# Kernel tuning notes

Hardware: AMD Instinct MI355X
Metric: run time of the kernel (lower is better)

The kernel has to match this reference:

```python
import jax, jax.numpy as jnp
import numpy as np

B, N, NID, V, GH, PHI, RHO = 8, 256, 64, 128, 128, 256, 128
BN = B * N
EPS = 1e-5


def _layernorm(x, g, b):
    m = jnp.mean(x, axis=-1, keepdims=True)
    v = jnp.var(x, axis=-1, keepdims=True)
    return (x - m) * jax.lax.rsqrt(v + EPS) * g + b


def _edges(A):
    # dense adjacency -> flat batched edge list, exactly as mask.nonzero() ordering
    bidx = jnp.arange(B)[:, None, None]
    ii = jnp.arange(N)[None, :, None]
    jj = jnp.arange(N)[None, None, :]
    src = jnp.broadcast_to(bidx * N + ii, (B, N, N)).reshape(-1)  # edge_index[0] = b*N+i
    tgt = jnp.broadcast_to(bidx * N + jj, (B, N, N)).reshape(-1)  # edge_index[1] = b*N+j
    w = A.reshape(-1)
    valid = w != 0
    rel = (w > 0).astype(jnp.int32)
    return src, tgt, w, valid, rel


def _rgcn(H, src, tgt, valid, rel, Wrel, Wroot, bias):
    # torch_geometric RGCNConv: mean aggregation per relation at target + root + bias
    x_src = H[src]  # (E, d) gather
    out = H @ Wroot + bias
    for r in range(2):
        m = (valid & (rel == r)).astype(H.dtype)  # (E,)
        s = jax.ops.segment_sum(x_src * m[:, None], tgt, num_segments=BN)
        c = jax.ops.segment_sum(m, tgt, num_segments=BN)
        out = out + (s / jnp.maximum(c, 1.0)[:, None]) @ Wrel[r]
    return out


def setup_inputs() -> dict:
    key = jax.random.key(0)
    ks = jax.random.split(key, 24)
    p = lambda k, shape: jax.random.normal(k, shape, dtype=jnp.float32) * 0.02
    z = lambda *shape: jnp.zeros(shape, jnp.float32)
    return {
        "A": jax.random.normal(ks[0], (B, N, N), dtype=jnp.float32),
        "X": jax.random.normal(ks[1], (B, N, NID), dtype=jnp.float32),
        "home_mask": (jax.random.uniform(ks[2], (B, N)) > 0.5).astype(jnp.float32),
        "emb1_w": p(ks[3], (NID, V)), "emb1_b": z(V),
        "emb2_w": p(ks[4], (V, V)), "emb2_b": z(V),
        "rgcn_w_0": p(ks[5], (2, V, GH)), "rgcn_root_0": p(ks[6], (V, GH)), "rgcn_bias_0": z(GH),
        "lina_w_0": p(ks[7], (GH, GH)), "lina_b_0": z(GH),
        "linb_w_0": p(ks[8], (GH, GH)), "linb_b_0": z(GH),
        "rgcn_w_1": p(ks[9], (2, GH, GH)), "rgcn_root_1": p(ks[10], (GH, GH)), "rgcn_bias_1": z(GH),
        "lina_w_1": p(ks[11], (GH, GH)), "lina_b_1": z(GH),
        "linb_w_1": p(ks[12], (GH, GH)), "linb_b_1": z(GH),
        "norm_g": jnp.ones((GH,), jnp.float32), "norm_b": z(GH),
        "phi_w1": p(ks[13], (GH, PHI)), "phi_b1": z(PHI),
        "phi_w2": p(ks[14], (PHI, PHI)), "phi_b2": z(PHI),
        "rho_w1": p(ks[15], (PHI, RHO)), "rho_b1": z(RHO),
        "rho_w2": p(ks[16], (RHO, 1)), "rho_b2": z(1),
    }


def reference(A, X, home_mask, emb1_w, emb1_b, emb2_w, emb2_b,
              rgcn_w_0, rgcn_root_0, rgcn_bias_0, lina_w_0, lina_b_0, linb_w_0, linb_b_0,
              rgcn_w_1, rgcn_root_1, rgcn_bias_1, lina_w_1, lina_b_1, linb_w_1, linb_b_1,
              norm_g, norm_b, phi_w1, phi_b1, phi_w2, phi_b2,
              rho_w1, rho_b1, rho_w2, rho_b2):
    away_mask = 1.0 - home_mask
    H = jax.nn.relu(X @ emb1_w + emb1_b)
    H = (H @ emb2_w + emb2_b).reshape(BN, V)

    src, tgt, w, valid, rel = _edges(A)
    aw = jnp.abs(w) * valid.astype(w.dtype)  # |edge_weight|, zero for masked-out edges

    blocks = [
        (rgcn_w_0, rgcn_root_0, rgcn_bias_0, lina_w_0, lina_b_0, linb_w_0, linb_b_0),
        (rgcn_w_1, rgcn_root_1, rgcn_bias_1, lina_w_1, lina_b_1, linb_w_1, linb_b_1),
    ]
    agg = jnp.zeros_like(H)
    for (Wrel, Wroot, bias, law, lab, lbw, lbb) in blocks:
        H = H + agg
        H2 = _rgcn(H, src, tgt, valid, rel, Wrel, Wroot, bias)
        # gather-scale-scatter: agg[src] += H2[tgt] * |w|
        agg = jax.ops.segment_sum(H2[tgt] * aw[:, None], src, num_segments=BN)
        agg = jax.nn.relu(_layernorm(agg, norm_g, norm_b))  # dropout = identity (eval)
        agg = jax.nn.relu(agg @ law + lab)
        agg = agg @ lbw + lbb
    H = (H + agg).reshape(B, N, GH)

    # DeepSet phi (dropout = identity)
    h = jax.nn.relu(H @ phi_w1 + phi_b1)
    phi_out = jax.nn.relu(h @ phi_w2 + phi_b2)  # (B, N, PHI)

    home_sum = jnp.sum(phi_out * home_mask[:, :, None], axis=1)
    away_sum = jnp.sum(phi_out * away_mask[:, :, None], axis=1)

    def rho(s):
        return (jax.nn.relu(s @ rho_w1 + rho_b1) @ rho_w2 + rho_b2)[:, 0]

    out = rho(home_sum) - rho(away_sum)
    return 0.5 + 0.5 * jnp.tanh(out)  # (B,)
```

## Files before the change

kernel.cpp:

```cpp
#include <hip/hip_runtime.h>
#include <math.h>

#define NB 8
#define NN 256
#define DV 128

typedef __attribute__((address_space(1))) const void* gas1p;
typedef __attribute__((address_space(3))) void* las3p;
static __device__ __forceinline__ void gld16(const float* g, float* l) {
    __builtin_amdgcn_global_load_lds((gas1p)g, (las3p)l, 16, 0, 0);
}

__global__ __launch_bounds__(256, 2) void k_embed(const float* __restrict__ X,
        const float* __restrict__ w1, const float* __restrict__ b1,
        const float* __restrict__ w2, const float* __restrict__ b2,
        float* __restrict__ H, float* __restrict__ pools) {
    const int r0 = blockIdx.x * 4;
    const int t = threadIdx.x, q = t & 31, u = t >> 5;
    __shared__ __align__(16) float pool[12288];
    __shared__ __align__(16) float xq[256];
    __shared__ __align__(16) float h1q[512];
    float* part = pool + 8192;
    if (blockIdx.x < 16) pools[blockIdx.x * 256 + t] = 0.f;
    #pragma unroll
    for (int rnd = 0; rnd < 8; ++rnd) {
        int idx = rnd * 256 + t;
        gld16(w1 + idx * 4, &pool[idx * 4]);
    }
    if (t < 64) {
        float4 v;
        v.x = X[(size_t)(r0 + 0) * 64 + t];
        v.y = X[(size_t)(r0 + 1) * 64 + t];
        v.z = X[(size_t)(r0 + 2) * 64 + t];
        v.w = X[(size_t)(r0 + 3) * 64 + t];
        *(float4*)&xq[t * 4] = v;
    }
    __syncthreads();
    {
        float acc[16];
        #pragma unroll
        for (int i = 0; i < 16; ++i) acc[i] = 0.f;
        #pragma unroll
        for (int kk = 0; kk < 8; ++kk) {
            int k = u * 8 + kk;
            float4 w4 = *(const float4*)&pool[k * 128 + q * 4];
            float wc[4] = {w4.x, w4.y, w4.z, w4.w};
            float4 x4 = *(const float4*)&xq[k * 4];
            float xr[4] = {x4.x, x4.y, x4.z, x4.w};
            #pragma unroll
            for (int r = 0; r < 4; ++r)
                #pragma unroll
                for (int c = 0; c < 4; ++c)
                    acc[r * 4 + c] = fmaf(xr[r], wc[c], acc[r * 4 + c]);
        }
        #pragma unroll
        for (int r = 0; r < 4; ++r)
            *(float4*)&part[u * 512 + r * 128 + q * 4] =
                make_float4(acc[r*4+0], acc[r*4+1], acc[r*4+2], acc[r*4+3]);
    }
    __syncthreads();
    #pragma unroll
    for (int rnd = 0; rnd < 4; ++rnd) {
        int idx = rnd * 256 + t;
        gld16(w2 + idx * 4, &pool[idx * 4]);
    }
    if (t < 128) {
        int r = t >> 5, fq = t & 31;
        float4 s = *(const float4*)&b1[fq * 4];
        #pragma unroll
        for (int uu = 0; uu < 8; ++uu) {
            float4 p = *(const float4*)&part[uu * 512 + r * 128 + fq * 4];
            s.x += p.x; s.y += p.y; s.z += p.z; s.w += p.w;
        }
        h1q[(fq * 4 + 0) * 4 + r] = fmaxf(s.x, 0.f);
        h1q[(fq * 4 + 1) * 4 + r] = fmaxf(s.y, 0.f);
        h1q[(fq * 4 + 2) * 4 + r] = fmaxf(s.z, 0.f);
        h1q[(fq * 4 + 3) * 4 + r] = fmaxf(s.w, 0.f);
    }
    __syncthreads();
    float a2[16];
    #pragma unroll
    for (int i = 0; i < 16; ++i) a2[i] = 0.f;
    #pragma unroll 1
    for (int kt = 0; kt < 4; ++kt) {
        const int buf = kt & 1;
        if (kt < 3) {
            #pragma unroll
            for (int rnd = 0; rnd < 4; ++rnd) {
                int idx = rnd * 256 + t;
                gld16(w2 + (kt + 1) * 4096 + idx * 4,
                      &pool[(buf ^ 1) * 4096 + idx * 4]);
            }
        }
        const float* wt = &pool[buf * 4096];
        #pragma unroll
        for (int kk = 0; kk < 4; ++kk) {
            int kl = u * 4 + kk;
            float4 w4 = *(const float4*)&wt[kl * 128 + q * 4];
            float wc[4] = {w4.x, w4.y, w4.z, w4.w};
            float4 h4 = *(const float4*)&h1q[(kt * 32 + kl) * 4];
            float hr[4] = {h4.x, h4.y, h4.z, h4.w};
            #pragma unroll
            for (int r = 0; r < 4; ++r)
                #pragma unroll
                for (int c = 0; c < 4; ++c)
                    a2[r * 4 + c] = fmaf(hr[r], wc[c], a2[r * 4 + c]);
        }
        __syncthreads();
    }
    #pragma unroll
    for (int r = 0; r < 4; ++r)
        *(float4*)&part[u * 512 + r * 128 + q * 4] =
            make_float4(a2[r*4+0], a2[r*4+1], a2[r*4+2], a2[r*4+3]);
    __syncthreads();
    if (t < 128) {
        int r = t >> 5, fq = t & 31;
        float4 s = *(const float4*)&b2[fq * 4];
        #pragma unroll
        for (int uu = 0; uu < 8; ++uu) {
            float4 p = *(const float4*)&part[uu * 512 + r * 128 + fq * 4];
            s.x += p.x; s.y += p.y; s.z += p.z; s.w += p.w;
        }
        *(float4*)&H[(size_t)(r0 + r) * 128 + fq * 4] = s;
    }
}

__global__ __launch_bounds__(256, 2) void k_gcn1(
        const float* __restrict__ A, const float* __restrict__ H,
        const float* __restrict__ Wrel, const float* __restrict__ Wroot,
        const float* __restrict__ bias, float* __restrict__ H2) {
    const int b  = blockIdx.x >> 6;
    const int j0 = (blockIdx.x & 63) * 4;
    const int t = threadIdx.x, q = t & 31, u = t >> 5;
    __shared__ __align__(16) float pool[12288];
    __shared__ __align__(16) float pb[1536];
    __shared__ float cntp[256];
    __shared__ float cnt[8];
    float* htile = pool;
    float* maskM = pool + 8192;
    float* part  = pool;
    const float* Ab = A + (size_t)b * 65536;
    const float* Hb = H + (size_t)b * 32768;
    const float* W0 = Wrel;
    const float* W1 = Wrel + 16384;

    #pragma unroll
    for (int rnd = 0; rnd < 4; ++rnd) {
        int idx = rnd * 256 + t;
        gld16(Hb + idx * 4, &htile[idx * 4]);
    }
    {
        float4 a = *(const float4*)(Ab + (size_t)t * 256 + j0);
        float4 m0, m1;
        m0.x = (a.x < 0.f) ? 1.f : 0.f; m1.x = (a.x > 0.f) ? 1.f : 0.f;
        m0.y = (a.y < 0.f) ? 1.f : 0.f; m1.y = (a.y > 0.f) ? 1.f : 0.f;
        m0.z = (a.z < 0.f) ? 1.f : 0.f; m1.z = (a.z > 0.f) ? 1.f : 0.f;
        m0.w = (a.w < 0.f) ? 1.f : 0.f; m1.w = (a.w > 0.f) ? 1.f : 0.f;
        *(float4*)&maskM[t * 8]     = m0;
        *(float4*)&maskM[t * 8 + 4] = m1;
    }
    __syncthreads();
    {
        int chunk = t >> 3, slot = t & 7;
        float c = 0.f;
        #pragma unroll
        for (int qq = 0; qq < 8; ++qq) c += maskM[(chunk * 8 + qq) * 8 + slot];
        cntp[slot * 32 + chunk] = c;
    }
    float acc0[16], acc1[16];
    #pragma unroll
    for (int i = 0; i < 16; ++i) { acc0[i] = 0.f; acc1[i] = 0.f; }
    #pragma unroll 1
    for (int tl = 0; tl < 8; ++tl) {
        const int buf = tl & 1;
        if (tl < 7) {
            #pragma unroll
            for (int rnd = 0; rnd < 4; ++rnd) {
                int idx = rnd * 256 + t;
                gld16(Hb + (tl + 1) * 4096 + idx * 4,
                      &htile[(buf ^ 1) * 4096 + idx * 4]);
            }
        }
        const float* hb = &htile[buf * 4096];
        #pragma unroll
        for (int ii = 0; ii < 4; ++ii) {
            int iL = u * 4 + ii;
            int i  = tl * 32 + iL;
            float4 h4 = *(const float4*)&hb[iL * 128 + q * 4];
            float hc[4] = {h4.x, h4.y, h4.z, h4.w};
            float4 m0 = *(const float4*)&maskM[i * 8];
            float4 m1 = *(const float4*)&maskM[i * 8 + 4];
            float mr0[4] = {m0.x, m0.y, m0.z, m0.w};
            float mr1[4] = {m1.x, m1.y, m1.z, m1.w};
            #pragma unroll
            for (int r = 0; r < 4; ++r)
                #pragma unroll
                for (int c = 0; c < 4; ++c) {
                    acc0[r * 4 + c] = fmaf(mr0[r], hc[c], acc0[r * 4 + c]);
                    acc1[r * 4 + c] = fmaf(mr1[r], hc[c], acc1[r * 4 + c]);
                }
        }
        __syncthreads();
    }
    #pragma unroll
    for (int r = 0; r < 4; ++r) {
        *(float4*)&part[u * 1024 + r * 128 + q * 4] =
            make_float4(acc0[r*4+0], acc0[r*4+1], acc0[r*4+2], acc0[r*4+3]);
        *(float4*)&part[u * 1024 + (4 + r) * 128 + q * 4] =
            make_float4(acc1[r*4+0], acc1[r*4+1], acc1[r*4+2], acc1[r*4+3]);
    }
    if (t < 8) {
        float s = 0.f;
        #pragma unroll
        for (int c = 0; c < 32; ++c) s += cntp[t * 32 + c];
        cnt[t] = s;
    }
    __syncthreads();
    {
        int slot = t >> 5, fq = t & 31;
        float4 s = make_float4(0.f, 0.f, 0.f, 0.f);
        #pragma unroll
        for (int uu = 0; uu < 8; ++uu) {
            float4 p = *(const float4*)&part[uu * 1024 + slot * 128 + fq * 4];
            s.x += p.x; s.y += p.y; s.z += p.z; s.w += p.w;
        }
        float rc = 1.f / fmaxf(cnt[slot], 1.f);
        pb[(fq * 4 + 0) * 12 + 4 + slot] = s.x * rc;
        pb[(fq * 4 + 1) * 12 + 4 + slot] = s.y * rc;
        pb[(fq * 4 + 2) * 12 + 4 + slot] = s.z * rc;
        pb[(fq * 4 + 3) * 12 + 4 + slot] = s.w * rc;
    }
    if (t < 128) {
        int r = t >> 5, fq = t & 31;
        float4 g4 = *(const float4*)(Hb + (size_t)(j0 + r) * 128 + fq * 4);
        pb[(fq * 4 + 0) * 12 + r] = g4.x;
        pb[(fq * 4 + 1) * 12 + r] = g4.y;
        pb[(fq * 4 + 2) * 12 + r] = g4.z;
        pb[(fq * 4 + 3) * 12 + r] = g4.w;
    }
    __syncthreads();
    #pragma unroll
    for (int rnd = 0; rnd < 6; ++rnd) {
        int idx = rnd * 256 + t;
        int mat = idx >> 9, rem = idx & 511;
        const float* Wm = (mat == 0) ? Wroot : ((mat == 1) ? W0 : W1);
        gld16(Wm + rem * 4, &pool[mat * 2048 + rem * 4]);
    }
    __syncthreads();
    float bcc[16];
    #pragma unroll
    for (int i = 0; i < 16; ++i) bcc[i] = 0.f;
    #pragma unroll 1
    for (int kt = 0; kt < 8; ++kt) {
        const int buf = kt & 1;
        if (kt < 7) {
            #pragma unroll
            for (int rnd = 0; rnd < 6; ++rnd) {
                int idx = rnd * 256 + t;
                int mat = idx >> 9, rem = idx & 511;
                const float* Wm = (mat == 0) ? Wroot : ((mat == 1) ? W0 : W1);
                gld16(Wm + (kt + 1) * 2048 + rem * 4,
                      &pool[(buf ^ 1) * 6144 + mat * 2048 + rem * 4]);
            }
        }
        const float* wt = &pool[buf * 6144];
        #pragma unroll
        for (int kk = 0; kk < 2; ++kk) {
            int kl = u * 2 + kk;
            int k  = kt * 16 + kl;
            float4 wr = *(const float4*)&wt[kl * 128 + q * 4];
            float4 wa = *(const float4*)&wt[2048 + kl * 128 + q * 4];
            float4 wb = *(const float4*)&wt[4096 + kl * 128 + q * 4];
            float wrc[4] = {wr.x, wr.y, wr.z, wr.w};
            float wac[4] = {wa.x, wa.y, wa.z, wa.w};
            float wbc[4] = {wb.x, wb.y, wb.z, wb.w};
            float4 hv = *(const float4*)&pb[k * 12];
            float4 q0 = *(const float4*)&pb[k * 12 + 4];
            float4 q1 = *(const float4*)&pb[k * 12 + 8];
            float hr[4] = {hv.x, hv.y, hv.z, hv.w};
            float m0r[4] = {q0.x, q0.y, q0.z, q0.w};
            float m1r[4] = {q1.x, q1.y, q1.z, q1.w};
            #pragma unroll
            for (int r = 0; r < 4; ++r)
                #pragma unroll
                for (int c = 0; c < 4; ++c) {
                    float v = bcc[r * 4 + c];
                    v = fmaf(hr[r], wrc[c], v);
                    v = fmaf(m0r[r], wac[c], v);
                    v = fmaf(m1r[r], wbc[c], v);
                    bcc[r * 4 + c] = v;
                }
        }
        __syncthreads();
    }
    float* bpart = pool;
    #pragma unroll
    for (int r = 0; r < 4; ++r)
        *(float4*)&bpart[u * 512 + r * 128 + q * 4] =
            make_float4(bcc[r*4+0], bcc[r*4+1], bcc[r*4+2], bcc[r*4+3]);
    __syncthreads();
    if (t < 128) {
        int r = t >> 5, fq = t & 31;
        float4 s = *(const float4*)&bias[fq * 4];
        #pragma unroll
        for (int uu = 0; uu < 8; ++uu) {
            float4 p = *(const float4*)&bpart[uu * 512 + r * 128 + fq * 4];
            s.x += p.x; s.y += p.y; s.z += p.z; s.w += p.w;
        }
        *(float4*)&H2[(size_t)(b * 256 + j0 + r) * 128 + fq * 4] = s;
    }
}

__global__ __launch_bounds__(256, 2) void k_gcn2(
        const float* __restrict__ A, const float* __restrict__ H2,
        const float* __restrict__ g, const float* __restrict__ bta,
        const float* __restrict__ law, const float* __restrict__ lab,
        const float* __restrict__ lbw, const float* __restrict__ lbb,
        float* __restrict__ H) {
    const int b  = blockIdx.x >> 6;
    const int i0 = (blockIdx.x & 63) * 4;
    const int t = threadIdx.x, q = t & 31, u = t >> 5;
    __shared__ __align__(16) float pool[9216];
    __shared__ __align__(16) float xq[512];
    __shared__ __align__(16) float uq[512];
    __shared__ float red[16];
    __shared__ float mi[8];
    float* tileb = pool;
    float* absA  = pool + 8192;
    float* part  = pool;
    const float* Ab  = A + (size_t)b * 65536;
    const float* H2b = H2 + (size_t)b * 32768;

    #pragma unroll
    for (int rnd = 0; rnd < 4; ++rnd) {
        int idx = rnd * 256 + t;
        gld16(H2b + idx * 4, &tileb[idx * 4]);
    }
    {
        float4 av;
        av.x = fabsf(Ab[(size_t)(i0 + 0) * 256 + t]);
        av.y = fabsf(Ab[(size_t)(i0 + 1) * 256 + t]);
        av.z = fabsf(Ab[(size_t)(i0 + 2) * 256 + t]);
        av.w = fabsf(Ab[(size_t)(i0 + 3) * 256 + t]);
        *(float4*)&absA[t * 4] = av;
    }
    __syncthreads();
    float acc[16];
    #pragma unroll
    for (int i = 0; i < 16; ++i) acc[i] = 0.f;
    #pragma unroll 1
    for (int tl = 0; tl < 8; ++tl) {
        const int buf = tl & 1;
        if (tl < 7) {
            #pragma unroll
            for (int rnd = 0; rnd < 4; ++rnd) {
                int idx = rnd * 256 + t;
                gld16(H2b + (tl + 1) * 4096 + idx * 4,
                      &tileb[(buf ^ 1) * 4096 + idx * 4]);
            }
        }
        const float* hb = &tileb[buf * 4096];
        #pragma unroll
        for (int jj = 0; jj < 4; ++jj) {
            int jL = u * 4 + jj;
            int j  = tl * 32 + jL;
            float4 h4 = *(const float4*)&hb[jL * 128 + q * 4];
            float hc[4] = {h4.x, h4.y, h4.z, h4.w};
            float4 a4 = *(const float4*)&absA[j * 4];
            float ar[4] = {a4.x, a4.y, a4.z, a4.w};
            #pragma unroll
            for (int r = 0; r < 4; ++r)
                #pragma unroll
                for (int c = 0; c < 4; ++c)
                    acc[r * 4 + c] = fmaf(ar[r], hc[c], acc[r * 4 + c]);
        }
        __syncthreads();
    }
    #pragma unroll
    for (int r = 0; r < 4; ++r)
        *(float4*)&part[u * 512 + r * 128 + q * 4] =
            make_float4(acc[r*4+0], acc[r*4+1], acc[r*4+2], acc[r*4+3]);
    __syncthreads();
    #pragma unroll
    for (int rnd = 0; rnd < 2; ++rnd) {
        int idx = rnd * 256 + t;
        gld16(law + idx * 4, &pool[4096 + idx * 4]);
    }
    float x[4] = {0.f, 0.f, 0.f, 0.f};
    if (t < 128) {
        const int wv2 = t >> 6;
        #pragma unroll
        for (int r = 0; r < 4; ++r) {
            float s = 0.f;
            #pragma unroll
            for (int uu = 0; uu < 8; ++uu) s += part[uu * 512 + r * 128 + t];
            x[r] = s;
        }
        #pragma unroll
        for (int r = 0; r < 4; ++r) {
            float s = x[r], s2 = x[r] * x[r];
            #pragma unroll
            for (int o = 32; o > 0; o >>= 1) {
                s  += __shfl_down(s, o, 64);
                s2 += __shfl_down(s2, o, 64);
            }
            if ((t & 63) == 0) {
                red[r * 4 + wv2 * 2] = s;
                red[r * 4 + wv2 * 2 + 1] = s2;
            }
        }
    }
    __syncthreads();
    if (t < 4) {
        float s  = red[t * 4] + red[t * 4 + 2];
        float s2 = red[t * 4 + 1] + red[t * 4 + 3];
        float m = s * (1.f / 128.f);
        float v = s2 * (1.f / 128.f) - m * m;
        mi[t * 2] = m;
        mi[t * 2 + 1] = rsqrtf(v + 1e-5f);
    }
    __syncthreads();
    if (t < 128) {
        float gf = g[t], bf = bta[t];
        float4 xv;
        xv.x = fmaxf((x[0] - mi[0]) * mi[1] * gf + bf, 0.f);
        xv.y = fmaxf((x[1] - mi[2]) * mi[3] * gf + bf, 0.f);
        xv.z = fmaxf((x[2] - mi[4]) * mi[5] * gf + bf, 0.f);
        xv.w = fmaxf((x[3] - mi[6]) * mi[7] * gf + bf, 0.f);
        *(float4*)&xq[t * 4] = xv;
    }
    __syncthreads();
    float u1[16];
    #pragma unroll
    for (int i = 0; i < 16; ++i) u1[i] = 0.f;
    #pragma unroll 1
    for (int kt = 0; kt < 8; ++kt) {
        const int buf = kt & 1;
        if (kt < 7) {
            #pragma unroll
            for (int rnd = 0; rnd < 2; ++rnd) {
                int idx = rnd * 256 + t;
                gld16(law + (kt + 1) * 2048 + idx * 4,
                      &pool[4096 + (buf ^ 1) * 2048 + idx * 4]);
            }
        }
        const float* wt = &pool[4096 + buf * 2048];
        #pragma unroll
        for (int kk = 0; kk < 2; ++kk) {
            int kl = u * 2 + kk;
            int k  = kt * 16 + kl;
            float4 w4 = *(const float4*)&wt[kl * 128 + q * 4];
            float wc[4] = {w4.x, w4.y, w4.z, w4.w};
            float4 x4 = *(const float4*)&xq[k * 4];
            float xr[4] = {x4.x, x4.y, x4.z, x4.w};
            #pragma unroll
            for (int r = 0; r < 4; ++r)
                #pragma unroll
                for (int c = 0; c < 4; ++c)
                    u1[r * 4 + c] = fmaf(xr[r], wc[c], u1[r * 4 + c]);
        }
        __syncthreads();
    }
    #pragma unroll
    for (int r = 0; r < 4; ++r)
        *(float4*)&part[u * 512 + r * 128 + q * 4] =
            make_float4(u1[r*4+0], u1[r*4+1], u1[r*4+2], u1[r*4+3]);
    __syncthreads();
    #pragma unroll
    for (int rnd = 0; rnd < 2; ++rnd) {
        int idx = rnd * 256 + t;
        gld16(lbw + idx * 4, &pool[4096 + idx * 4]);
    }
    if (t < 128) {
        float bb = lab[t];
        float4 uv;
        float s0 = 0.f, s1 = 0.f, s2 = 0.f, s3 = 0.f;
        #pragma unroll
        for (int uu = 0; uu < 8; ++uu) {
            s0 += part[uu * 512 + 0 * 128 + t];
            s1 += part[uu * 512 + 1 * 128 + t];
            s2 += part[uu * 512 + 2 * 128 + t];
            s3 += part[uu * 512 + 3 * 128 + t];
        }
        uv.x = fmaxf(s0 + bb, 0.f);
        uv.y = fmaxf(s1 + bb, 0.f);
        uv.z = fmaxf(s2 + bb, 0.f);
        uv.w = fmaxf(s3 + bb, 0.f);
        *(float4*)&uq[t * 4] = uv;
    }
    __syncthreads();
    float u2[16];
    #pragma unroll
    for (int i = 0; i < 16; ++i) u2[i] = 0.f;
    #pragma unroll 1
    for (int kt = 0; kt < 8; ++kt) {
        const int buf = kt & 1;
        if (kt < 7) {
            #pragma unroll
            for (int rnd = 0; rnd < 2; ++rnd) {
                int idx = rnd * 256 + t;
                gld16(lbw + (kt + 1) * 2048 + idx * 4,
                      &pool[4096 + (buf ^ 1) * 2048 + idx * 4]);
            }
        }
        const float* wt = &pool[4096 + buf * 2048];
        #pragma unroll
        for (int kk = 0; kk < 2; ++kk) {
            int kl = u * 2 + kk;
            int k  = kt * 16 + kl;
            float4 w4 = *(const float4*)&wt[kl * 128 + q * 4];
            float wc[4] = {w4.x, w4.y, w4.z, w4.w};
            float4 x4 = *(const float4*)&uq[k * 4];
            float xr[4] = {x4.x, x4.y, x4.z, x4.w};
            #pragma unroll
            for (int r = 0; r < 4; ++r)
                #pragma unroll
                for (int c = 0; c < 4; ++c)
                    u2[r * 4 + c] = fmaf(xr[r], wc[c], u2[r * 4 + c]);
        }
        __syncthreads();
    }
    #pragma unroll
    for (int r = 0; r < 4; ++r)
        *(float4*)&part[u * 512 + r * 128 + q * 4] =
            make_float4(u2[r*4+0], u2[r*4+1], u2[r*4+2], u2[r*4+3]);
    __syncthreads();
    if (t < 128) {
        int r = t >> 5, fq = t & 31;
        float4 s = *(const float4*)&lbb[fq * 4];
        #pragma unroll
        for (int uu = 0; uu < 8; ++uu) {
            float4 p = *(const float4*)&part[uu * 512 + r * 128 + fq * 4];
            s.x += p.x; s.y += p.y; s.z += p.z; s.w += p.w;
        }
        float4 hold = *(const float4*)(H + (size_t)(b * 256 + i0 + r) * 128 + fq * 4);
        s.x += hold.x; s.y += hold.y; s.z += hold.z; s.w += hold.w;
        *(float4*)&H[(size_t)(b * 256 + i0 + r) * 128 + fq * 4] = s;
    }
}

__global__ __launch_bounds__(256) void k_deepset(
        const float* __restrict__ H, const float* __restrict__ hm,
        const float* __restrict__ w1, const float* __restrict__ b1,
        const float* __restrict__ w2, const float* __restrict__ b2,
        float* __restrict__ hsum, float* __restrict__ asum) {
    const int r0 = blockIdx.x * 8;
    const int b  = blockIdx.x >> 5;
    const int t  = threadIdx.x, q = t & 63, u = t >> 6;
    __shared__ __align__(16) float wt2[2][8192];
    __shared__ __align__(16) float part[8192];
    __shared__ __align__(16) float hraw[1024];
    __shared__ __align__(16) float ph2[2048];
    __shared__ float hmv[8];
    #pragma unroll
    for (int rnd = 0; rnd < 8; ++rnd) {
        int idx = rnd * 256 + t;
        gld16(w1 + idx * 4, &wt2[0][idx * 4]);
    }
    gld16(H + (size_t)r0 * 128 + t * 4, &hraw[t * 4]);
    if (t < 8) hmv[t] = hm[r0 + t];
    __syncthreads();
    float acc[32];
    #pragma unroll
    for (int i = 0; i < 32; ++i) acc[i] = 0.f;
    #pragma unroll 1
    for (int kt = 0; kt < 4; ++kt) {
        const int buf = kt & 1;
        if (kt < 3) {
            #pragma unroll
            for (int rnd = 0; rnd < 8; ++rnd) {
                int idx = rnd * 256 + t;
                gld16(w1 + (kt + 1) * 8192 + idx * 4, &wt2[buf ^ 1][idx * 4]);
            }
        }
        const float* wt = wt2[buf];
        #pragma unroll
        for (int kk = 0; kk < 8; ++kk) {
            int kl = u * 8 + kk;
            int k  = kt * 32 + kl;
            float4 w4 = *(const float4*)&wt[kl * 256 + q * 4];
            float wc[4] = {w4.x, w4.y, w4.z, w4.w};
            float hr[8];
            #pragma unroll
            for (int r = 0; r < 8; ++r) hr[r] = hraw[r * 128 + k];
            #pragma unroll
            for (int r = 0; r < 8; ++r)
                #pragma unroll
                for (int c = 0; c < 4; ++c)
                    acc[r * 4 + c] = fmaf(hr[r], wc[c], acc[r * 4 + c]);
        }
        __syncthreads();
    }
    #pragma unroll
    for (int r = 0; r < 8; ++r)
        *(float4*)&part[u * 2048 + r * 256 + q * 4] =
            make_float4(acc[r*4+0], acc[r*4+1], acc[r*4+2], acc[r*4+3]);
    __syncthreads();
    #pragma unroll
    for (int rnd = 0; rnd < 8; ++rnd) {
        int idx = rnd * 256 + t;
        gld16(w2 + idx * 4, &wt2[0][idx * 4]);
    }
    #pragma unroll
    for (int e = 0; e < 2; ++e) {
        int idx = e * 256 + t;
        int r = idx >> 6, fq = idx & 63;
        float4 s = *(const float4*)&b1[fq * 4];
        #pragma unroll
        for (int uu = 0; uu < 4; ++uu) {
            float4 p = *(const float4*)&part[uu * 2048 + r * 256 + fq * 4];
            s.x += p.x; s.y += p.y; s.z += p.z; s.w += p.w;
        }
        s.x = fmaxf(s.x, 0.f); s.y = fmaxf(s.y, 0.f);
        s.z = fmaxf(s.z, 0.f); s.w = fmaxf(s.w, 0.f);
        *(float4*)&ph2[r * 256 + fq * 4] = s;
    }
    __syncthreads();
    float a2[32];
    #pragma unroll
    for (int i = 0; i < 32; ++i) a2[i] = 0.f;
    #pragma unroll 1
    for (int kt = 0; kt < 8; ++kt) {
        const int buf = kt & 1;
        if (kt < 7) {
            #pragma unroll
            for (int rnd = 0; rnd < 8; ++rnd) {
                int idx = rnd * 256 + t;
                gld16(w2 + (kt + 1) * 8192 + idx * 4, &wt2[buf ^ 1][idx * 4]);
            }
        }
        const float* wt = wt2[buf];
        #pragma unroll
        for (int kk = 0; kk < 8; ++kk) {
            int kl = u * 8 + kk;
            int k  = kt * 32 + kl;
            float4 w4 = *(const float4*)&wt[kl * 256 + q * 4];
            float wc[4] = {w4.x, w4.y, w4.z, w4.w};
            float pr[8];
            #pragma unroll
            for (int r = 0; r < 8; ++r) pr[r] = ph2[r * 256 + k];
            #pragma unroll
            for (int r = 0; r < 8; ++r)
                #pragma unroll
                for (int c = 0; c < 4; ++c)
                    a2[r * 4 + c] = fmaf(pr[r], wc[c], a2[r * 4 + c]);
        }
        __syncthreads();
    }
    #pragma unroll
    for (int r = 0; r < 8; ++r)
        *(float4*)&part[u * 2048 + r * 256 + q * 4] =
            make_float4(a2[r*4+0], a2[r*4+1], a2[r*4+2], a2[r*4+3]);
    __syncthreads();
    {
        float bb = b2[t];
        float hp = 0.f, sp = 0.f;
        #pragma unroll
        for (int r = 0; r < 8; ++r) {
            float s = bb;
            #pragma unroll
            for (int uu = 0; uu < 4; ++uu) s += part[uu * 2048 + r * 256 + t];
            float p = fmaxf(s, 0.f);
            sp += p;
            hp = fmaf(p, hmv[r], hp);
        }
        atomicAdd(&hsum[b * 256 + t], hp);
        atomicAdd(&asum[b * 256 + t], sp - hp);
    }
}

__global__ __launch_bounds__(256) void k_rho(const float* __restrict__ hsum,
        const float* __restrict__ asum,
        const float* __restrict__ w1, const float* __restrict__ b1,
        const float* __restrict__ w2, const float* __restrict__ b2,
        float* __restrict__ out) {
    const int bIdx = blockIdx.x;
    const int t = threadIdx.x, q = t & 31, u = t >> 5;
    __shared__ __align__(16) float pool[10240];
    __shared__ __align__(16) float sv[512];
    __shared__ float wsv[2];
    float* part = pool + 8192;
    #pragma unroll
    for (int rnd = 0; rnd < 4; ++rnd) {
        int idx = rnd * 256 + t;
        gld16(w1 + idx * 4, &pool[idx * 4]);
    }
    sv[t] = hsum[bIdx * 256 + t];
    sv[256 + t] = asum[bIdx * 256 + t];
    __syncthreads();
    float aH[4] = {0.f, 0.f, 0.f, 0.f}, aA[4] = {0.f, 0.f, 0.f, 0.f};
    #pragma unroll 1
    for (int kt = 0; kt < 8; ++kt) {
        const int buf = kt & 1;
        if (kt < 7) {
            #pragma unroll
            for (int rnd = 0; rnd < 4; ++rnd) {
                int idx = rnd * 256 + t;
                gld16(w1 + (kt + 1) * 4096 + idx * 4,
                      &pool[(buf ^ 1) * 4096 + idx * 4]);
            }
        }
        const float* wt = &pool[buf * 4096];
        #pragma unroll
        for (int kk = 0; kk < 4; ++kk) {
            int kl = u * 4 + kk;
            int k  = kt * 32 + kl;
            float4 w4 = *(const float4*)&wt[kl * 128 + q * 4];
            float sh = sv[k], sa = sv[256 + k];
            aH[0] = fmaf(sh, w4.x, aH[0]); aA[0] = fmaf(sa, w4.x, aA[0]);
            aH[1] = fmaf(sh, w4.y, aH[1]); aA[1] = fmaf(sa, w4.y, aA[1]);
            aH[2] = fmaf(sh, w4.z, aH[2]); aA[2] = fmaf(sa, w4.z, aA[2]);
            aH[3] = fmaf(sh, w4.w, aH[3]); aA[3] = fmaf(sa, w4.w, aA[3]);
        }
        __syncthreads();
    }
    *(float4*)&part[u * 256 + q * 4]       = make_float4(aH[0], aH[1], aH[2], aH[3]);
    *(float4*)&part[u * 256 + 128 + q * 4] = make_float4(aA[0], aA[1], aA[2], aA[3]);
    __syncthreads();
    if (t < 64) {
        int vec = t >> 5, fq = t & 31;
        float4 s = make_float4(0.f, 0.f, 0.f, 0.f);
        #pragma unroll
        for (int uu = 0; uu < 8; ++uu) {
            float4 p = *(const float4*)&part[uu * 256 + vec * 128 + fq * 4];
            s.x += p.x; s.y += p.y; s.z += p.z; s.w += p.w;
        }
        float4 bb = *(const float4*)&b1[fq * 4];
        float4 w2q = *(const float4*)&w2[fq * 4];
        float p = fmaxf(s.x + bb.x, 0.f) * w2q.x
                + fmaxf(s.y + bb.y, 0.f) * w2q.y
                + fmaxf(s.z + bb.z, 0.f) * w2q.z
                + fmaxf(s.w + bb.w, 0.f) * w2q.w;
        #pragma unroll
        for (int o = 16; o > 0; o >>= 1) p += __shfl_down(p, o, 32);
        if ((t & 31) == 0) wsv[vec] = p;
    }
    __syncthreads();
    if (t == 0) out[bIdx] = 0.5f + 0.5f * tanhf(wsv[0] - wsv[1]);
}

extern "C" void kernel_launch(void* const* d_in, const int* in_sizes, int n_in,
                              void* d_out, int out_size, void* d_ws, size_t ws_size,
                              hipStream_t stream) {
    const float* A         = (const float*)d_in[0];
    const float* X         = (const float*)d_in[1];
    const float* home_mask = (const float*)d_in[2];
    const float* emb1_w    = (const float*)d_in[3];
    const float* emb1_b    = (const float*)d_in[4];
    const float* emb2_w    = (const float*)d_in[5];
    const float* emb2_b    = (const float*)d_in[6];
    const float* rgcn_w[2]    = { (const float*)d_in[7],  (const float*)d_in[14] };
    const float* rgcn_root[2] = { (const float*)d_in[8],  (const float*)d_in[15] };
    const float* rgcn_bias[2] = { (const float*)d_in[9],  (const float*)d_in[16] };
    const float* lina_w[2]    = { (const float*)d_in[10], (const float*)d_in[17] };
    const float* lina_b[2]    = { (const float*)d_in[11], (const float*)d_in[18] };
    const float* linb_w[2]    = { (const float*)d_in[12], (const float*)d_in[19] };
    const float* linb_b[2]    = { (const float*)d_in[13], (const float*)d_in[20] };
    const float* norm_g  = (const float*)d_in[21];
    const float* norm_b  = (const float*)d_in[22];
    const float* phi_w1  = (const float*)d_in[23];
    const float* phi_b1  = (const float*)d_in[24];
    const float* phi_w2  = (const float*)d_in[25];
    const float* phi_b2  = (const float*)d_in[26];
    const float* rho_w1  = (const float*)d_in[27];
    const float* rho_b1  = (const float*)d_in[28];
    const float* rho_w2  = (const float*)d_in[29];
    const float* rho_b2  = (const float*)d_in[30];
    float* out = (float*)d_out;

    float* ws   = (float*)d_ws;
    float* H    = ws;
    float* H2   = ws + 262144;
    float* hsum = ws + 524288;
    float* asum = ws + 526336;

    k_embed<<<512, 256, 0, stream>>>(X, emb1_w, emb1_b, emb2_w, emb2_b, H, hsum);

    for (int it = 0; it < 2; ++it) {
        k_gcn1<<<512, 256, 0, stream>>>(A, H, rgcn_w[it], rgcn_root[it],
                                        rgcn_bias[it], H2);
        k_gcn2<<<512, 256, 0, stream>>>(A, H2, norm_g, norm_b,
                                        lina_w[it], lina_b[it],
                                        linb_w[it], linb_b[it], H);
    }

    k_deepset<<<256, 256, 0, stream>>>(H, home_mask, phi_w1, phi_b1,
                                       phi_w2, phi_b2, hsum, asum);
    k_rho<<<NB, 256, 0, stream>>>(hsum, asum, rho_w1, rho_b1, rho_w2, rho_b2, out);
}
```

Measured before the change: 207.1 us.

## Fuse all stages into one persistent kernel with software grid barriers

Replaces the six separate kernel launches with an init kernel plus a single persistent 256-block kernel whose stages are separated by atomic-counter grid barriers. The GCN stages now process 8 target columns per block instead of 4, which doubles the register tiles and halves the block count. The aim is to remove launch gaps and inter-kernel drain. The cost is barrier spin latency, lower parallelism, and reliance on all 256 blocks being co-resident on the device.

New measurement: 301.8 us. +45.8%, slower.

```diff
diff --git a/kernel.cpp b/kernel.cpp
--- a/kernel.cpp
+++ b/kernel.cpp
@@ -2,8 +2,7 @@
 #include <math.h>
 
 #define NB 8
-#define NN 256
-#define DV 128
+#define GRID 256
 
 typedef __attribute__((address_space(1))) const void* gas1p;
 typedef __attribute__((address_space(3))) void* las3p;
@@ -11,165 +10,82 @@
     __builtin_amdgcn_global_load_lds((gas1p)g, (las3p)l, 16, 0, 0);
 }
 
-__global__ __launch_bounds__(256, 2) void k_embed(const float* __restrict__ X,
-        const float* __restrict__ w1, const float* __restrict__ b1,
-        const float* __restrict__ w2, const float* __restrict__ b2,
-        float* __restrict__ H, float* __restrict__ pools) {
-    const int r0 = blockIdx.x * 4;
-    const int t = threadIdx.x, q = t & 31, u = t >> 5;
-    __shared__ __align__(16) float pool[12288];
-    __shared__ __align__(16) float xq[256];
-    __shared__ __align__(16) float h1q[512];
-    float* part = pool + 8192;
-    if (blockIdx.x < 16) pools[blockIdx.x * 256 + t] = 0.f;
-    #pragma unroll
-    for (int rnd = 0; rnd < 8; ++rnd) {
-        int idx = rnd * 256 + t;
-        gld16(w1 + idx * 4, &pool[idx * 4]);
-    }
-    if (t < 64) {
-        float4 v;
-        v.x = X[(size_t)(r0 + 0) * 64 + t];
-        v.y = X[(size_t)(r0 + 1) * 64 + t];
-        v.z = X[(size_t)(r0 + 2) * 64 + t];
-        v.w = X[(size_t)(r0 + 3) * 64 + t];
-        *(float4*)&xq[t * 4] = v;
-    }
-    __syncthreads();
+struct Params {
+    const float *A, *X, *hm;
+    const float *e1w, *e1b, *e2w, *e2b;
+    const float *rw0, *rr0, *rb0, *law0, *lab0, *lbw0, *lbb0;
+    const float *rw1, *rr1, *rb1, *law1, *lab1, *lbw1, *lbb1;
+    const float *ng, *nbta;
+    const float *pw1, *pb1, *pw2, *pb2;
+    const float *qw1, *qb1, *qw2, *qb2;
+    float *H, *H2, *hsum, *asum, *outp;
+    int *cnt;
+};
+
+__global__ __launch_bounds__(256) void k_init(float* pools, int* cnt) {
+    int i = blockIdx.x * 256 + threadIdx.x;
+    if (i < 4096) pools[i] = 0.f;
+    if (blockIdx.x == 16 && threadIdx.x < 16) cnt[threadIdx.x] = 0;
+}
+
+__device__ __forceinline__ void gridbar(int* cnt, int id) {
+    __syncthreads();
+    if (threadIdx.x == 0) {
+        __threadfence();
+        __hip_atomic_fetch_add(&cnt[id], 1, __ATOMIC_RELAXED, __HIP_MEMORY_SCOPE_AGENT);
+        while (__hip_atomic_load(&cnt[id], __ATOMIC_RELAXED,
+                                 __HIP_MEMORY_SCOPE_AGENT) < GRID)
+            __builtin_amdgcn_s_sleep(4);
+        __threadfence();
+    }
+    __syncthreads();
+}
+
+__device__ void stage_gcn1(float* S, const float* Ab, const float* Hb,
+        const float* Wrel, const float* Wroot, const float* bias,
+        float* H2b, int j0, int t, int q, int u) {
+    float* ldsM = S;
+    float* ht   = S + 4096;
+    float* part = S + 4096;
+    float* pb   = S + 12288;
+    float* Wt   = S;
+    float* cntp = S + 15360;
+    float* cnt  = S + 15616;
+    const float* W0 = Wrel;
+    const float* W1 = Wrel + 16384;
+
     {
-        float acc[16];
-        #pragma unroll
-        for (int i = 0; i < 16; ++i) acc[i] = 0.f;
-        #pragma unroll
-        for (int kk = 0; kk < 8; ++kk) {
-            int k = u * 8 + kk;
-            float4 w4 = *(const float4*)&pool[k * 128 + q * 4];
-            float wc[4] = {w4.x, w4.y, w4.z, w4.w};
-            float4 x4 = *(const float4*)&xq[k * 4];
-            float xr[4] = {x4.x, x4.y, x4.z, x4.w};
-            #pragma unroll
-            for (int r = 0; r < 4; ++r)
-                #pragma unroll
-                for (int c = 0; c < 4; ++c)
-                    acc[r * 4 + c] = fmaf(xr[r], wc[c], acc[r * 4 + c]);
-        }
-        #pragma unroll
-        for (int r = 0; r < 4; ++r)
-            *(float4*)&part[u * 512 + r * 128 + q * 4] =
-                make_float4(acc[r*4+0], acc[r*4+1], acc[r*4+2], acc[r*4+3]);
-    }
-    __syncthreads();
+        float4 a0 = *(const float4*)(Ab + (size_t)t * 256 + j0);
+        float4 a1 = *(const float4*)(Ab + (size_t)t * 256 + j0 + 4);
+        *(float4*)&ldsM[t * 16] = make_float4(
+            (a0.x < 0.f) ? 1.f : 0.f, (a0.y < 0.f) ? 1.f : 0.f,
+            (a0.z < 0.f) ? 1.f : 0.f, (a0.w < 0.f) ? 1.f : 0.f);
+        *(float4*)&ldsM[t * 16 + 4] = make_float4(
+            (a1.x < 0.f) ? 1.f : 0.f, (a1.y < 0.f) ? 1.f : 0.f,
+            (a1.z < 0.f) ? 1.f : 0.f, (a1.w < 0.f) ? 1.f : 0.f);
+        *(float4*)&ldsM[t * 16 + 8] = make_float4(
+            (a0.x > 0.f) ? 1.f : 0.f, (a0.y > 0.f) ? 1.f : 0.f,
+            (a0.z > 0.f) ? 1.f : 0.f, (a0.w > 0.f) ? 1.f : 0.f);
+        *(float4*)&ldsM[t * 16 + 12] = make_float4(
+            (a1.x > 0.f) ? 1.f : 0.f, (a1.y > 0.f) ? 1.f : 0.f,
+            (a1.z > 0.f) ? 1.f : 0.f, (a1.w > 0.f) ? 1.f : 0.f);
+    }
     #pragma unroll
     for (int rnd = 0; rnd < 4; ++rnd) {
         int idx = rnd * 256 + t;
-        gld16(w2 + idx * 4, &pool[idx * 4]);
-    }
-    if (t < 128) {
-        int r = t >> 5, fq = t & 31;
-        float4 s = *(const float4*)&b1[fq * 4];
-        #pragma unroll
-        for (int uu = 0; uu < 8; ++uu) {
-            float4 p = *(const float4*)&part[uu * 512 + r * 128 + fq * 4];
-            s.x += p.x; s.y += p.y; s.z += p.z; s.w += p.w;
-        }
-        h1q[(fq * 4 + 0) * 4 + r] = fmaxf(s.x, 0.f);
-        h1q[(fq * 4 + 1) * 4 + r] = fmaxf(s.y, 0.f);
-        h1q[(fq * 4 + 2) * 4 + r] = fmaxf(s.z, 0.f);
-        h1q[(fq * 4 + 3) * 4 + r] = fmaxf(s.w, 0.f);
-    }
-    __syncthreads();
-    float a2[16];
-    #pragma unroll
-    for (int i = 0; i < 16; ++i) a2[i] = 0.f;
-    #pragma unroll 1
-    for (int kt = 0; kt < 4; ++kt) {
-        const int buf = kt & 1;
-        if (kt < 3) {
-            #pragma unroll
-            for (int rnd = 0; rnd < 4; ++rnd) {
-                int idx = rnd * 256 + t;
-                gld16(w2 + (kt + 1) * 4096 + idx * 4,
-                      &pool[(buf ^ 1) * 4096 + idx * 4]);
-            }
-        }
-        const float* wt = &pool[buf * 4096];
-        #pragma unroll
-        for (int kk = 0; kk < 4; ++kk) {
-            int kl = u * 4 + kk;
-            float4 w4 = *(const float4*)&wt[kl * 128 + q * 4];
-            float wc[4] = {w4.x, w4.y, w4.z, w4.w};
-            float4 h4 = *(const float4*)&h1q[(kt * 32 + kl) * 4];
-            float hr[4] = {h4.x, h4.y, h4.z, h4.w};
-            #pragma unroll
-            for (int r = 0; r < 4; ++r)
-                #pragma unroll
-                for (int c = 0; c < 4; ++c)
-                    a2[r * 4 + c] = fmaf(hr[r], wc[c], a2[r * 4 + c]);
-        }
-        __syncthreads();
-    }
-    #pragma unroll
-    for (int r = 0; r < 4; ++r)
-        *(float4*)&part[u * 512 + r * 128 + q * 4] =
-            make_float4(a2[r*4+0], a2[r*4+1], a2[r*4+2], a2[r*4+3]);
-    __syncthreads();
-    if (t < 128) {
-        int r = t >> 5, fq = t & 31;
-        float4 s = *(const float4*)&b2[fq * 4];
-        #pragma unroll
-        for (int uu = 0; uu < 8; ++uu) {
-            float4 p = *(const float4*)&part[uu * 512 + r * 128 + fq * 4];
-            s.x += p.x; s.y += p.y; s.z += p.z; s.w += p.w;
-        }
-        *(float4*)&H[(size_t)(r0 + r) * 128 + fq * 4] = s;
-    }
-}
-
-__global__ __launch_bounds__(256, 2) void k_gcn1(
-        const float* __restrict__ A, const float* __restrict__ H,
-        const float* __restrict__ Wrel, const float* __restrict__ Wroot,
-        const float* __restrict__ bias, float* __restrict__ H2) {
-    const int b  = blockIdx.x >> 6;
-    const int j0 = (blockIdx.x & 63) * 4;
-    const int t = threadIdx.x, q = t & 31, u = t >> 5;
-    __shared__ __align__(16) float pool[12288];
-    __shared__ __align__(16) float pb[1536];
-    __shared__ float cntp[256];
-    __shared__ float cnt[8];
-    float* htile = pool;
-    float* maskM = pool + 8192;
-    float* part  = pool;
-    const float* Ab = A + (size_t)b * 65536;
-    const float* Hb = H + (size_t)b * 32768;
-    const float* W0 = Wrel;
-    const float* W1 = Wrel + 16384;
-
-    #pragma unroll
-    for (int rnd = 0; rnd < 4; ++rnd) {
-        int idx = rnd * 256 + t;
-        gld16(Hb + idx * 4, &htile[idx * 4]);
-    }
+        gld16(Hb + idx * 4, &ht[idx * 4]);
+    }
+    __syncthreads();
     {
-        float4 a = *(const float4*)(Ab + (size_t)t * 256 + j0);
-        float4 m0, m1;
-        m0.x = (a.x < 0.f) ? 1.f : 0.f; m1.x = (a.x > 0.f) ? 1.f : 0.f;
-        m0.y = (a.y < 0.f) ? 1.f : 0.f; m1.y = (a.y > 0.f) ? 1.f : 0.f;
-        m0.z = (a.z < 0.f) ? 1.f : 0.f; m1.z = (a.z > 0.f) ? 1.f : 0.f;
-        m0.w = (a.w < 0.f) ? 1.f : 0.f; m1.w = (a.w > 0.f) ? 1.f : 0.f;
-        *(float4*)&maskM[t * 8]     = m0;
-        *(float4*)&maskM[t * 8 + 4] = m1;
-    }
-    __syncthreads();
-    {
-        int chunk = t >> 3, slot = t & 7;
+        int chunk = t >> 4, slot = t & 15;
         float c = 0.f;
         #pragma unroll
-        for (int qq = 0; qq < 8; ++qq) c += maskM[(chunk * 8 + qq) * 8 + slot];
-        cntp[slot * 32 + chunk] = c;
-    }
-    float acc0[16], acc1[16];
-    #pragma unroll
-    for (int i = 0; i < 16; ++i) { acc0[i] = 0.f; acc1[i] = 0.f; }
+        for (int qq = 0; qq < 16; ++qq) c += ldsM[(chunk * 16 + qq) * 16 + slot];
+        cntp[slot * 16 + chunk] = c;
+    }
+    float acc0[32], acc1[32];
+    #pragma unroll
+    for (int i = 0; i < 32; ++i) { acc0[i] = 0.f; acc1[i] = 0.f; }
     #pragma unroll 1
     for (int tl = 0; tl < 8; ++tl) {
         const int buf = tl & 1;
@@ -177,23 +93,24 @@
             #pragma unroll
             for (int rnd = 0; rnd < 4; ++rnd) {
                 int idx = rnd * 256 + t;
-                gld16(Hb + (tl + 1) * 4096 + idx * 4,
-                      &htile[(buf ^ 1) * 4096 + idx * 4]);
-            }
-        }
-        const float* hb = &htile[buf * 4096];
+                gld16(Hb + (tl + 1) * 4096 + idx * 4, &ht[(buf ^ 1) * 4096 + idx * 4]);
+            }
+        }
+        const float* hb = &ht[buf * 4096];
         #pragma unroll
         for (int ii = 0; ii < 4; ++ii) {
             int iL = u * 4 + ii;
             int i  = tl * 32 + iL;
             float4 h4 = *(const float4*)&hb[iL * 128 + q * 4];
             float hc[4] = {h4.x, h4.y, h4.z, h4.w};
-            float4 m0 = *(const float4*)&maskM[i * 8];
-            float4 m1 = *(const float4*)&maskM[i * 8 + 4];
-            float mr0[4] = {m0.x, m0.y, m0.z, m0.w};
-            float mr1[4] = {m1.x, m1.y, m1.z, m1.w};
-            #pragma unroll
-            for (int r = 0; r < 4; ++r)
+            float4 m0a = *(const float4*)&ldsM[i * 16];
+            float4 m0b = *(const float4*)&ldsM[i * 16 + 4];
+            float4 m1a = *(const float4*)&ldsM[i * 16 + 8];
+            float4 m1b = *(const float4*)&ldsM[i * 16 + 12];
+            float mr0[8] = {m0a.x, m0a.y, m0a.z, m0a.w, m0b.x, m0b.y, m0b.z, m0b.w};
+            float mr1[8] = {m1a.x, m1a.y, m1a.z, m1a.w, m1b.x, m1b.y, m1b.z, m1b.w};
+            #pragma unroll
+            for (int r = 0; r < 8; ++r)
                 #pragma unroll
                 for (int c = 0; c < 4; ++c) {
                     acc0[r * 4 + c] = fmaf(mr0[r], hc[c], acc0[r * 4 + c]);
@@ -202,41 +119,46 @@
         }
         __syncthreads();
     }
-    #pragma unroll
-    for (int r = 0; r < 4; ++r) {
+    if (t < 16) {
+        float s = 0.f;
+        #pragma unroll
+        for (int c = 0; c < 16; ++c) s += cntp[t * 16 + c];
+        cnt[t] = s;
+    }
+    #pragma unroll
+    for (int e = 0; e < 4; ++e) {
+        int idx = e * 256 + t;
+        int r = idx >> 7, k = idx & 127;
+        pb[k * 24 + r] = Hb[(size_t)(j0 + r) * 128 + k];
+    }
+    #pragma unroll
+    for (int r = 0; r < 8; ++r)
         *(float4*)&part[u * 1024 + r * 128 + q * 4] =
             make_float4(acc0[r*4+0], acc0[r*4+1], acc0[r*4+2], acc0[r*4+3]);
-        *(float4*)&part[u * 1024 + (4 + r) * 128 + q * 4] =
+    __syncthreads();
+    #pragma unroll
+    for (int e = 0; e < 4; ++e) {
+        int idx = e * 256 + t;
+        int r = idx >> 7, k = idx & 127;
+        float s = 0.f;
+        #pragma unroll
+        for (int uu = 0; uu < 8; ++uu) s += part[uu * 1024 + r * 128 + k];
+        pb[k * 24 + 8 + r] = s / fmaxf(cnt[r], 1.f);
+    }
+    __syncthreads();
+    #pragma unroll
+    for (int r = 0; r < 8; ++r)
+        *(float4*)&part[u * 1024 + r * 128 + q * 4] =
             make_float4(acc1[r*4+0], acc1[r*4+1], acc1[r*4+2], acc1[r*4+3]);
-    }
-    if (t < 8) {
+    __syncthreads();
+    #pragma unroll
+    for (int e = 0; e < 4; ++e) {
+        int idx = e * 256 + t;
+        int r = idx >> 7, k = idx & 127;
         float s = 0.f;
         #pragma unroll
-        for (int c = 0; c < 32; ++c) s += cntp[t * 32 + c];
-        cnt[t] = s;
-    }
-    __syncthreads();
-    {
-        int slot = t >> 5, fq = t & 31;
-        float4 s = make_float4(0.f, 0.f, 0.f, 0.f);
-        #pragma unroll
-        for (int uu = 0; uu < 8; ++uu) {
-            float4 p = *(const float4*)&part[uu * 1024 + slot * 128 + fq * 4];
-            s.x += p.x; s.y += p.y; s.z += p.z; s.w += p.w;
-        }
-        float rc = 1.f / fmaxf(cnt[slot], 1.f);
-        pb[(fq * 4 + 0) * 12 + 4 + slot] = s.x * rc;
-        pb[(fq * 4 + 1) * 12 + 4 + slot] = s.y * rc;
-        pb[(fq * 4 + 2) * 12 + 4 + slot] = s.z * rc;
-        pb[(fq * 4 + 3) * 12 + 4 + slot] = s.w * rc;
-    }
-    if (t < 128) {
-        int r = t >> 5, fq = t & 31;
-        float4 g4 = *(const float4*)(Hb + (size_t)(j0 + r) * 128 + fq * 4);
-        pb[(fq * 4 + 0) * 12 + r] = g4.x;
-        pb[(fq * 4 + 1) * 12 + r] = g4.y;
-        pb[(fq * 4 + 2) * 12 + r] = g4.z;
-        pb[(fq * 4 + 3) * 12 + r] = g4.w;
+        for (int uu = 0; uu < 8; ++uu) s += part[uu * 1024 + r * 128 + k];
+        pb[k * 24 + 16 + r] = s / fmaxf(cnt[8 + r], 1.f);
     }
     __syncthreads();
     #pragma unroll
@@ -244,12 +166,12 @@
         int idx = rnd * 256 + t;
         int mat = idx >> 9, rem = idx & 511;
         const float* Wm = (mat == 0) ? Wroot : ((mat == 1) ? W0 : W1);
-        gld16(Wm + rem * 4, &pool[mat * 2048 + rem * 4]);
-    }
-    __syncthreads();
-    float bcc[16];
-    #pragma unroll
-    for (int i = 0; i < 16; ++i) bcc[i] = 0.f;
+        gld16(Wm + rem * 4, &Wt[mat * 2048 + rem * 4]);
+    }
+    __syncthreads();
+    float bcc[32];
+    #pragma unroll
+    for (int i = 0; i < 32; ++i) bcc[i] = 0.f;
     #pragma unroll 1
     for (int kt = 0; kt < 8; ++kt) {
         const int buf = kt & 1;
@@ -260,28 +182,29 @@
                 int mat = idx >> 9, rem = idx & 511;
                 const float* Wm = (mat == 0) ? Wroot : ((mat == 1) ? W0 : W1);
                 gld16(Wm + (kt + 1) * 2048 + rem * 4,
-                      &pool[(buf ^ 1) * 6144 + mat * 2048 + rem * 4]);
-            }
-        }
-        const float* wt = &pool[buf * 6144];
+                      &Wt[(buf ^ 1) * 6144 + mat * 2048 + rem * 4]);
+            }
+        }
+        const float* wt = &Wt[buf * 6144];
         #pragma unroll
         for (int kk = 0; kk < 2; ++kk) {
             int kl = u * 2 + kk;
             int k  = kt * 16 + kl;
-            float4 wr = *(const float4*)&wt[kl * 128 + q * 4];
-            float4 wa = *(const float4*)&wt[2048 + kl * 128 + q * 4];
-            float4 wb = *(const float4*)&wt[4096 + kl * 128 + q * 4];
-            float wrc[4] = {wr.x, wr.y, wr.z, wr.w};
-            float wac[4] = {wa.x, wa.y, wa.z, wa.w};
-            float wbc[4] = {wb.x, wb.y, wb.z, wb.w};
-            float4 hv = *(const float4*)&pb[k * 12];
-            float4 q0 = *(const float4*)&pb[k * 12 + 4];
-            float4 q1 = *(const float4*)&pb[k * 12 + 8];
-            float hr[4] = {hv.x, hv.y, hv.z, hv.w};
-            float m0r[4] = {q0.x, q0.y, q0.z, q0.w};
-            float m1r[4] = {q1.x, q1.y, q1.z, q1.w};
-            #pragma unroll
-            for (int r = 0; r < 4; ++r)
+            float4 wr4 = *(const float4*)&wt[kl * 128 + q * 4];
+            float4 wa4 = *(const float4*)&wt[2048 + kl * 128 + q * 4];
+            float4 wb4 = *(const float4*)&wt[4096 + kl * 128 + q * 4];
+            float wrc[4] = {wr4.x, wr4.y, wr4.z, wr4.w};
+            float wac[4] = {wa4.x, wa4.y, wa4.z, wa4.w};
+            float wbc[4] = {wb4.x, wb4.y, wb4.z, wb4.w};
+            const float* pk = &pb[k * 24];
+            float4 hA = *(const float4*)pk,        hB = *(const float4*)(pk + 4);
+            float4 qA = *(const float4*)(pk + 8),  qB = *(const float4*)(pk + 12);
+            float4 rA = *(const float4*)(pk + 16), rB = *(const float4*)(pk + 20);
+            float hr[8]  = {hA.x, hA.y, hA.z, hA.w, hB.x, hB.y, hB.z, hB.w};
+            float m0r[8] = {qA.x, qA.y, qA.z, qA.w, qB.x, qB.y, qB.z, qB.w};
+            float m1r[8] = {rA.x, rA.y, rA.z, rA.w, rB.x, rB.y, rB.z, rB.w};
+            #pragma unroll
+            for (int r = 0; r < 8; ++r)
                 #pragma unroll
                 for (int c = 0; c < 4; ++c) {
                     float v = bcc[r * 4 + c];
@@ -293,61 +216,52 @@
         }
         __syncthreads();
     }
-    float* bpart = pool;
-    #pragma unroll
-    for (int r = 0; r < 4; ++r)
-        *(float4*)&bpart[u * 512 + r * 128 + q * 4] =
+    float* bpart = S;
+    #pragma unroll
+    for (int r = 0; r < 8; ++r)
+        *(float4*)&bpart[u * 1024 + r * 128 + q * 4] =
             make_float4(bcc[r*4+0], bcc[r*4+1], bcc[r*4+2], bcc[r*4+3]);
     __syncthreads();
-    if (t < 128) {
-        int r = t >> 5, fq = t & 31;
-        float4 s = *(const float4*)&bias[fq * 4];
-        #pragma unroll
-        for (int uu = 0; uu < 8; ++uu) {
-            float4 p = *(const float4*)&bpart[uu * 512 + r * 128 + fq * 4];
-            s.x += p.x; s.y += p.y; s.z += p.z; s.w += p.w;
-        }
-        *(float4*)&H2[(size_t)(b * 256 + j0 + r) * 128 + fq * 4] = s;
-    }
+    #pragma unroll
+    for (int e = 0; e < 4; ++e) {
+        int idx = e * 256 + t;
+        int r = idx >> 7, f = idx & 127;
+        float s = bias[f];
+        #pragma unroll
+        for (int uu = 0; uu < 8; ++uu) s += bpart[uu * 1024 + r * 128 + f];
+        H2b[(size_t)(j0 + r) * 128 + f] = s;
+    }
+    __syncthreads();
 }
 
-__global__ __launch_bounds__(256, 2) void k_gcn2(
-        const float* __restrict__ A, const float* __restrict__ H2,
-        const float* __restrict__ g, const float* __restrict__ bta,
-        const float* __restrict__ law, const float* __restrict__ lab,
-        const float* __restrict__ lbw, const float* __restrict__ lbb,
-        float* __restrict__ H) {
-    const int b  = blockIdx.x >> 6;
-    const int i0 = (blockIdx.x & 63) * 4;
-    const int t = threadIdx.x, q = t & 31, u = t >> 5;
-    __shared__ __align__(16) float pool[9216];
-    __shared__ __align__(16) float xq[512];
-    __shared__ __align__(16) float uq[512];
-    __shared__ float red[16];
-    __shared__ float mi[8];
-    float* tileb = pool;
-    float* absA  = pool + 8192;
-    float* part  = pool;
-    const float* Ab  = A + (size_t)b * 65536;
-    const float* H2b = H2 + (size_t)b * 32768;
-
+__device__ void stage_gcn2(float* S, const float* Ab, const float* H2b,
+        const float* g, const float* bta, const float* law, const float* lab,
+        const float* lbw, const float* lbb, float* Hb, int i0, int t, int q, int u) {
+    float* absA = S;
+    float* ht   = S + 2048;
+    float* part = S + 2048;
+    float* xq   = S + 10240;
+    float* uq   = S + 11264;
+    float* Wt   = S + 12288;
+    float* red  = S + 16384;
+    float* mi   = S + 16416;
+
+    {
+        float v[8];
+        #pragma unroll
+        for (int r = 0; r < 8; ++r) v[r] = fabsf(Ab[(size_t)(i0 + r) * 256 + t]);
+        *(float4*)&absA[t * 8]     = make_float4(v[0], v[1], v[2], v[3]);
+        *(float4*)&absA[t * 8 + 4] = make_float4(v[4], v[5], v[6], v[7]);
+    }
     #pragma unroll
     for (int rnd = 0; rnd < 4; ++rnd) {
         int idx = rnd * 256 + t;
-        gld16(H2b + idx * 4, &tileb[idx * 4]);
-    }
-    {
-        float4 av;
-        av.x = fabsf(Ab[(size_t)(i0 + 0) * 256 + t]);
-        av.y = fabsf(Ab[(size_t)(i0 + 1) * 256 + t]);
-        av.z = fabsf(Ab[(size_t)(i0 + 2) * 256 + t]);
-        av.w = fabsf(Ab[(size_t)(i0 + 3) * 256 + t]);
-        *(float4*)&absA[t * 4] = av;
-    }
-    __syncthreads();
-    float acc[16];
-    #pragma unroll
-    for (int i = 0; i < 16; ++i) acc[i] = 0.f;
+        gld16(H2b + idx * 4, &ht[idx * 4]);
+    }
+    __syncthreads();
+    float acc[32];
+    #pragma unroll
+    for (int i = 0; i < 32; ++i) acc[i] = 0.f;
     #pragma unroll 1
     for (int tl = 0; tl < 8; ++tl) {
         const int buf = tl & 1;
@@ -355,21 +269,21 @@
             #pragma unroll
             for (int rnd = 0; rnd < 4; ++rnd) {
                 int idx = rnd * 256 + t;
-                gld16(H2b + (tl + 1) * 4096 + idx * 4,
-                      &tileb[(buf ^ 1) * 4096 + idx * 4]);
-            }
-        }
-        const float* hb = &tileb[buf * 4096];
+                gld16(H2b + (tl + 1) * 4096 + idx * 4, &ht[(buf ^ 1) * 4096 + idx * 4]);
+            }
+        }
+        const float* hb = &ht[buf * 4096];
         #pragma unroll
         for (int jj = 0; jj < 4; ++jj) {
             int jL = u * 4 + jj;
             int j  = tl * 32 + jL;
             float4 h4 = *(const float4*)&hb[jL * 128 + q * 4];
             float hc[4] = {h4.x, h4.y, h4.z, h4.w};
-            float4 a4 = *(const float4*)&absA[j * 4];
-            float ar[4] = {a4.x, a4.y, a4.z, a4.w};
-            #pragma unroll
-            for (int r = 0; r < 4; ++r)
+            float4 aA = *(const float4*)&absA[j * 8];
+            float4 aB = *(const float4*)&absA[j * 8 + 4];
+            float ar[8] = {aA.x, aA.y, aA.z, aA.w, aB.x, aB.y, aB.z, aB.w};
+            #pragma unroll
+            for (int r = 0; r < 8; ++r)
                 #pragma unroll
                 for (int c = 0; c < 4; ++c)
                     acc[r * 4 + c] = fmaf(ar[r], hc[c], acc[r * 4 + c]);
@@ -377,41 +291,38 @@
         __syncthreads();
     }
     #pragma unroll
-    for (int r = 0; r < 4; ++r)
-        *(float4*)&part[u * 512 + r * 128 + q * 4] =
+    for (int r = 0; r < 8; ++r)
+        *(float4*)&part[u * 1024 + r * 128 + q * 4] =
             make_float4(acc[r*4+0], acc[r*4+1], acc[r*4+2], acc[r*4+3]);
-    __syncthreads();
     #pragma unroll
     for (int rnd = 0; rnd < 2; ++rnd) {
         int idx = rnd * 256 + t;
-        gld16(law + idx * 4, &pool[4096 + idx * 4]);
-    }
-    float x[4] = {0.f, 0.f, 0.f, 0.f};
+        gld16(law + idx * 4, &Wt[idx * 4]);
+    }
+    __syncthreads();
+    float x[8];
     if (t < 128) {
-        const int wv2 = t >> 6;
-        #pragma unroll
-        for (int r = 0; r < 4; ++r) {
+        const int wv = t >> 6;
+        #pragma unroll
+        for (int r = 0; r < 8; ++r) {
             float s = 0.f;
             #pragma unroll
-            for (int uu = 0; uu < 8; ++uu) s += part[uu * 512 + r * 128 + t];
+            for (int uu = 0; uu < 8; ++uu) s += part[uu * 1024 + r * 128 + t];
             x[r] = s;
         }
         #pragma unroll
-        for (int r = 0; r < 4; ++r) {
+        for (int r = 0; r < 8; ++r) {
             float s = x[r], s2 = x[r] * x[r];
             #pragma unroll
             for (int o = 32; o > 0; o >>= 1) {
                 s  += __shfl_down(s, o, 64);
                 s2 += __shfl_down(s2, o, 64);
             }
-            if ((t & 63) == 0) {
-                red[r * 4 + wv2 * 2] = s;
-                red[r * 4 + wv2 * 2 + 1] = s2;
-            }
-        }
-    }
-    __syncthreads();
-    if (t < 4) {
+            if ((t & 63) == 0) { red[r * 4 + wv * 2] = s; red[r * 4 + wv * 2 + 1] = s2; }
+        }
+    }
+    __syncthreads();
+    if (t < 8) {
         float s  = red[t * 4] + red[t * 4 + 2];
         float s2 = red[t * 4 + 1] + red[t * 4 + 3];
         float m = s * (1.f / 128.f);
@@ -422,17 +333,14 @@
     __syncthreads();
     if (t < 128) {
         float gf = g[t], bf = bta[t];
-        float4 xv;
-        xv.x = fmaxf((x[0] - mi[0]) * mi[1] * gf + bf, 0.f);
-        xv.y = fmaxf((x[1] - mi[2]) * mi[3] * gf + bf, 0.f);
-        xv.z = fmaxf((x[2] - mi[4]) * mi[5] * gf + bf, 0.f);
-        xv.w = fmaxf((x[3] - mi[6]) * mi[7] * gf + bf, 0.f);
-        *(float4*)&xq[t * 4] = xv;
-    }
-    __syncthreads();
-    float u1[16];
-    #pragma unroll
-    for (int i = 0; i < 16; ++i) u1[i] = 0.f;
+        #pragma unroll
+        for (int r = 0; r < 8; ++r)
+            xq[t * 8 + r] = fmaxf((x[r] - mi[r * 2]) * mi[r * 2 + 1] * gf + bf, 0.f);
+    }
+    __syncthreads();
+    float u1[32];
+    #pragma unroll
+    for (int i = 0; i < 32; ++i) u1[i] = 0.f;
     #pragma unroll 1
     for (int kt = 0; kt < 8; ++kt) {
         const int buf = kt & 1;
@@ -440,21 +348,21 @@
             #pragma unroll
             for (int rnd = 0; rnd < 2; ++rnd) {
                 int idx = rnd * 256 + t;
-                gld16(law + (kt + 1) * 2048 + idx * 4,
-                      &pool[4096 + (buf ^ 1) * 2048 + idx * 4]);
-            }
-        }
-        const float* wt = &pool[4096 + buf * 2048];
+                gld16(law + (kt + 1) * 2048 + idx * 4, &Wt[(buf ^ 1) * 2048 + idx * 4]);
+            }
+        }
+        const float* wt = &Wt[buf * 2048];
         #pragma unroll
         for (int kk = 0; kk < 2; ++kk) {
             int kl = u * 2 + kk;
             int k  = kt * 16 + kl;
             float4 w4 = *(const float4*)&wt[kl * 128 + q * 4];
             float wc[4] = {w4.x, w4.y, w4.z, w4.w};
-            float4 x4 = *(const float4*)&xq[k * 4];
-            float xr[4] = {x4.x, x4.y, x4.z, x4.w};
-            #pragma unroll
-            for (int r = 0; r < 4; ++r)
+            float4 xA = *(const float4*)&xq[k * 8];
+            float4 xB = *(const float4*)&xq[k * 8 + 4];
+            float xr[8] = {xA.x, xA.y, xA.z, xA.w, xB.x, xB.y, xB.z, xB.w};
+            #pragma unroll
+            for (int r = 0; r < 8; ++r)
                 #pragma unroll
                 for (int c = 0; c < 4; ++c)
                     u1[r * 4 + c] = fmaf(xr[r], wc[c], u1[r * 4 + c]);
@@ -462,36 +370,29 @@
         __syncthreads();
     }
     #pragma unroll
-    for (int r = 0; r < 4; ++r)
-        *(float4*)&part[u * 512 + r * 128 + q * 4] =
+    for (int r = 0; r < 8; ++r)
+        *(float4*)&part[u * 1024 + r * 128 + q * 4] =
             make_float4(u1[r*4+0], u1[r*4+1], u1[r*4+2], u1[r*4+3]);
-    __syncthreads();
     #pragma unroll
     for (int rnd = 0; rnd < 2; ++rnd) {
         int idx = rnd * 256 + t;
-        gld16(lbw + idx * 4, &pool[4096 + idx * 4]);
-    }
+        gld16(lbw + idx * 4, &Wt[idx * 4]);
+    }
+    __syncthreads();
     if (t < 128) {
         float bb = lab[t];
-        float4 uv;
-        float s0 = 0.f, s1 = 0.f, s2 = 0.f, s3 = 0.f;
-        #pragma unroll
-        for (int uu = 0; uu < 8; ++uu) {
-            s0 += part[uu * 512 + 0 * 128 + t];
-            s1 += part[uu * 512 + 1 * 128 + t];
-            s2 += part[uu * 512 + 2 * 128 + t];
-            s3 += part[uu * 512 + 3 * 128 + t];
-        }
-        uv.x = fmaxf(s0 + bb, 0.f);
-        uv.y = fmaxf(s1 + bb, 0.f);
-        uv.z = fmaxf(s2 + bb, 0.f);
-        uv.w = fmaxf(s3 + bb, 0.f);
-        *(float4*)&uq[t * 4] = uv;
-    }
-    __syncthreads();
-    float u2[16];
-    #pragma unroll
-    for (int i = 0; i < 16; ++i) u2[i] = 0.f;
+        #pragma unroll
+        for (int r = 0; r < 8; ++r) {
+            float s = bb;
+            #pragma unroll
+            for (int uu = 0; uu < 8; ++uu) s += part[uu * 1024 + r * 128 + t];
+            uq[t * 8 + r] = fmaxf(s, 0.f);
+        }
+    }
+    __syncthreads();
+    float u2[32];
+    #pragma unroll
+    for (int i = 0; i < 32; ++i) u2[i] = 0.f;
     #pragma unroll 1
     for (int kt = 0; kt < 8; ++kt) {
         const int buf = kt & 1;
@@ -499,21 +400,21 @@
             #pragma unroll
             for (int rnd = 0; rnd < 2; ++rnd) {
                 int idx = rnd * 256 + t;
-                gld16(lbw + (kt + 1) * 2048 + idx * 4,
-                      &pool[4096 + (buf ^ 1) * 2048 + idx * 4]);
-            }
-        }
-        const float* wt = &pool[4096 + buf * 2048];
+                gld16(lbw + (kt + 1) * 2048 + idx * 4, &Wt[(buf ^ 1) * 2048 + idx * 4]);
+            }
+        }
+        const float* wt = &Wt[buf * 2048];
         #pragma unroll
         for (int kk = 0; kk < 2; ++kk) {
             int kl = u * 2 + kk;
             int k  = kt * 16 + kl;
             float4 w4 = *(const float4*)&wt[kl * 128 + q * 4];
             float wc[4] = {w4.x, w4.y, w4.z, w4.w};
-            float4 x4 = *(const float4*)&uq[k * 4];
-            float xr[4] = {x4.x, x4.y, x4.z, x4.w};
-            #pragma unroll
-            for (int r = 0; r < 4; ++r)
+            float4 xA = *(const float4*)&uq[k * 8];
+            float4 xB = *(const float4*)&uq[k * 8 + 4];
+            float xr[8] = {xA.x, xA.y, xA.z, xA.w, xB.x, xB.y, xB.z, xB.w};
+            #pragma unroll
+            for (int r = 0; r < 8; ++r)
                 #pragma unroll
                 for (int c = 0; c < 4; ++c)
                     u2[r * 4 + c] = fmaf(xr[r], wc[c], u2[r * 4 + c]);
@@ -521,270 +422,392 @@
         __syncthreads();
     }
     #pragma unroll
-    for (int r = 0; r < 4; ++r)
-        *(float4*)&part[u * 512 + r * 128 + q * 4] =
+    for (int r = 0; r < 8; ++r)
+        *(float4*)&part[u * 1024 + r * 128 + q * 4] =
             make_float4(u2[r*4+0], u2[r*4+1], u2[r*4+2], u2[r*4+3]);
     __syncthreads();
-    if (t < 128) {
-        int r = t >> 5, fq = t & 31;
-        float4 s = *(const float4*)&lbb[fq * 4];
-        #pragma unroll
-        for (int uu = 0; uu < 8; ++uu) {
-            float4 p = *(const float4*)&part[uu * 512 + r * 128 + fq * 4];
-            s.x += p.x; s.y += p.y; s.z += p.z; s.w += p.w;
-        }
-        float4 hold = *(const float4*)(H + (size_t)(b * 256 + i0 + r) * 128 + fq * 4);
-        s.x += hold.x; s.y += hold.y; s.z += hold.z; s.w += hold.w;
-        *(float4*)&H[(size_t)(b * 256 + i0 + r) * 128 + fq * 4] = s;
-    }
+    #pragma unroll
+    for (int e = 0; e < 4; ++e) {
+        int idx = e * 256 + t;
+        int r = idx >> 7, f = idx & 127;
+        float s = lbb[f];
+        #pragma unroll
+        for (int uu = 0; uu < 8; ++uu) s += part[uu * 1024 + r * 128 + f];
+        size_t o = (size_t)(i0 + r) * 128 + f;
+        Hb[o] = Hb[o] + s;
+    }
+    __syncthreads();
 }
 
-__global__ __launch_bounds__(256) void k_deepset(
-        const float* __restrict__ H, const float* __restrict__ hm,
-        const float* __restrict__ w1, const float* __restrict__ b1,
-        const float* __restrict__ w2, const float* __restrict__ b2,
-        float* __restrict__ hsum, float* __restrict__ asum) {
-    const int r0 = blockIdx.x * 8;
-    const int b  = blockIdx.x >> 5;
-    const int t  = threadIdx.x, q = t & 63, u = t >> 6;
-    __shared__ __align__(16) float wt2[2][8192];
-    __shared__ __align__(16) float part[8192];
-    __shared__ __align__(16) float hraw[1024];
-    __shared__ __align__(16) float ph2[2048];
-    __shared__ float hmv[8];
-    #pragma unroll
-    for (int rnd = 0; rnd < 8; ++rnd) {
-        int idx = rnd * 256 + t;
-        gld16(w1 + idx * 4, &wt2[0][idx * 4]);
-    }
-    gld16(H + (size_t)r0 * 128 + t * 4, &hraw[t * 4]);
-    if (t < 8) hmv[t] = hm[r0 + t];
-    __syncthreads();
-    float acc[32];
-    #pragma unroll
-    for (int i = 0; i < 32; ++i) acc[i] = 0.f;
-    #pragma unroll 1
-    for (int kt = 0; kt < 4; ++kt) {
-        const int buf = kt & 1;
-        if (kt < 3) {
-            #pragma unroll
-            for (int rnd = 0; rnd < 8; ++rnd) {
-                int idx = rnd * 256 + t;
-                gld16(w1 + (kt + 1) * 8192 + idx * 4, &wt2[buf ^ 1][idx * 4]);
-            }
-        }
-        const float* wt = wt2[buf];
+__global__ __launch_bounds__(256) void k_mega(Params P) {
+    __shared__ __align__(16) float S[21504];
+    const int blk = blockIdx.x;
+    const int t = threadIdx.x, q = t & 31, u = t >> 5;
+    const int b  = blk >> 5;
+    const int c0 = (blk & 31) * 8;
+    const int r0 = blk * 8;
+
+    {
+        float* w1s = S;
+        float* part = S;
+        float* h1q = S + 8192;
+        float* w2t = S + 9216;
+        float* xq  = S + 13312;
+        #pragma unroll
+        for (int rnd = 0; rnd < 8; ++rnd) {
+            int idx = rnd * 256 + t;
+            gld16(P.e1w + idx * 4, &w1s[idx * 4]);
+        }
+        #pragma unroll
+        for (int e = 0; e < 2; ++e) {
+            int idx = e * 256 + t;
+            int k = idx >> 3, r = idx & 7;
+            xq[k * 8 + r] = P.X[(size_t)(r0 + r) * 64 + k];
+        }
+        __syncthreads();
+        float acc[32];
+        #pragma unroll
+        for (int i = 0; i < 32; ++i) acc[i] = 0.f;
         #pragma unroll
         for (int kk = 0; kk < 8; ++kk) {
-            int kl = u * 8 + kk;
-            int k  = kt * 32 + kl;
-            float4 w4 = *(const float4*)&wt[kl * 256 + q * 4];
+            int k = u * 8 + kk;
+            float4 w4 = *(const float4*)&w1s[k * 128 + q * 4];
             float wc[4] = {w4.x, w4.y, w4.z, w4.w};
-            float hr[8];
-            #pragma unroll
-            for (int r = 0; r < 8; ++r) hr[r] = hraw[r * 128 + k];
+            float4 xA = *(const float4*)&xq[k * 8];
+            float4 xB = *(const float4*)&xq[k * 8 + 4];
+            float xr[8] = {xA.x, xA.y, xA.z, xA.w, xB.x, xB.y, xB.z, xB.w};
             #pragma unroll
             for (int r = 0; r < 8; ++r)
                 #pragma unroll
                 for (int c = 0; c < 4; ++c)
-                    acc[r * 4 + c] = fmaf(hr[r], wc[c], acc[r * 4 + c]);
-        }
-        __syncthreads();
-    }
-    #pragma unroll
-    for (int r = 0; r < 8; ++r)
-        *(float4*)&part[u * 2048 + r * 256 + q * 4] =
-            make_float4(acc[r*4+0], acc[r*4+1], acc[r*4+2], acc[r*4+3]);
-    __syncthreads();
-    #pragma unroll
-    for (int rnd = 0; rnd < 8; ++rnd) {
-        int idx = rnd * 256 + t;
-        gld16(w2 + idx * 4, &wt2[0][idx * 4]);
-    }
-    #pragma unroll
-    for (int e = 0; e < 2; ++e) {
-        int idx = e * 256 + t;
-        int r = idx >> 6, fq = idx & 63;
-        float4 s = *(const float4*)&b1[fq * 4];
-        #pragma unroll
-        for (int uu = 0; uu < 4; ++uu) {
-            float4 p = *(const float4*)&part[uu * 2048 + r * 256 + fq * 4];
-            s.x += p.x; s.y += p.y; s.z += p.z; s.w += p.w;
-        }
-        s.x = fmaxf(s.x, 0.f); s.y = fmaxf(s.y, 0.f);
-        s.z = fmaxf(s.z, 0.f); s.w = fmaxf(s.w, 0.f);
-        *(float4*)&ph2[r * 256 + fq * 4] = s;
-    }
-    __syncthreads();
-    float a2[32];
-    #pragma unroll
-    for (int i = 0; i < 32; ++i) a2[i] = 0.f;
-    #pragma unroll 1
-    for (int kt = 0; kt < 8; ++kt) {
-        const int buf = kt & 1;
-        if (kt < 7) {
-            #pragma unroll
-            for (int rnd = 0; rnd < 8; ++rnd) {
-                int idx = rnd * 256 + t;
-                gld16(w2 + (kt + 1) * 8192 + idx * 4, &wt2[buf ^ 1][idx * 4]);
-            }
-        }
-        const float* wt = wt2[buf];
-        #pragma unroll
-        for (int kk = 0; kk < 8; ++kk) {
-            int kl = u * 8 + kk;
-            int k  = kt * 32 + kl;
-            float4 w4 = *(const float4*)&wt[kl * 256 + q * 4];
-            float wc[4] = {w4.x, w4.y, w4.z, w4.w};
-            float pr[8];
-            #pragma unroll
-            for (int r = 0; r < 8; ++r) pr[r] = ph2[r * 256 + k];
-            #pragma unroll
-            for (int r = 0; r < 8; ++r)
-                #pragma unroll
-                for (int c = 0; c < 4; ++c)
-                    a2[r * 4 + c] = fmaf(pr[r], wc[c], a2[r * 4 + c]);
-        }
-        __syncthreads();
-    }
-    #pragma unroll
-    for (int r = 0; r < 8; ++r)
-        *(float4*)&part[u * 2048 + r * 256 + q * 4] =
-            make_float4(a2[r*4+0], a2[r*4+1], a2[r*4+2], a2[r*4+3]);
-    __syncthreads();
+                    acc[r * 4 + c] = fmaf(xr[r], wc[c], acc[r * 4 + c]);
+        }
+        __syncthreads();
+        #pragma unroll
+        for (int r = 0; r < 8; ++r)
+            *(float4*)&part[u * 1024 + r * 128 + q * 4] =
+                make_float4(acc[r*4+0], acc[r*4+1], acc[r*4+2], acc[r*4+3]);
+        #pragma unroll
+        for (int rnd = 0; rnd < 2; ++rnd) {
+            int idx = rnd * 256 + t;
+            gld16(P.e2w + idx * 4, &w2t[idx * 4]);
+        }
+        __syncthreads();
+        #pragma unroll
+        for (int e = 0; e < 4; ++e) {
+            int idx = e * 256 + t;
+            int f = idx >> 3, r = idx & 7;
+            float s = P.e1b[f];
+            #pragma unroll
+            for (int uu = 0; uu < 8; ++uu) s += part[uu * 1024 + r * 128 + f];
+            h1q[f * 8 + r] = fmaxf(s, 0.f);
+        }
+        __syncthreads();
+        float a2[32];
+        #pragma unroll
+        for (int i = 0; i < 32; ++i) a2[i] = 0.f;
+        #pragma unroll 1
+        for (int kt = 0; kt < 8; ++kt) {
+            const int buf = kt & 1;
+            if (kt < 7) {
+                #pragma unroll
+                for (int rnd = 0; rnd < 2; ++rnd) {
+                    int idx = rnd * 256 + t;
+                    gld16(P.e2w + (kt + 1) * 2048 + idx * 4,
+                          &w2t[(buf ^ 1) * 2048 + idx * 4]);
+                }
+            }
+            const float* wt = &w2t[buf * 2048];
+            #pragma unroll
+            for (int kk = 0; kk < 2; ++kk) {
+                int kl = u * 2 + kk;
+                int k  = kt * 16 + kl;
+                float4 w4 = *(const float4*)&wt[kl * 128 + q * 4];
+                float wc[4] = {w4.x, w4.y, w4.z, w4.w};
+                float4 hA = *(const float4*)&h1q[k * 8];
+                float4 hB = *(const float4*)&h1q[k * 8 + 4];
+                float hr[8] = {hA.x, hA.y, hA.z, hA.w, hB.x, hB.y, hB.z, hB.w};
+                #pragma unroll
+                for (int r = 0; r < 8; ++r)
+                    #pragma unroll
+                    for (int c = 0; c < 4; ++c)
+                        a2[r * 4 + c] = fmaf(hr[r], wc[c], a2[r * 4 + c]);
+            }
+            __syncthreads();
+        }
+        #pragma unroll
+        for (int r = 0; r < 8; ++r)
+            *(float4*)&part[u * 1024 + r * 128 + q * 4] =
+                make_float4(a2[r*4+0], a2[r*4+1], a2[r*4+2], a2[r*4+3]);
+        __syncthreads();
+        #pragma unroll
+        for (int e = 0; e < 4; ++e) {
+            int idx = e * 256 + t;
+            int r = idx >> 7, f = idx & 127;
+            float s = P.e2b[f];
+            #pragma unroll
+            for (int uu = 0; uu < 8; ++uu) s += part[uu * 1024 + r * 128 + f];
+            P.H[(size_t)(r0 + r) * 128 + f] = s;
+        }
+    }
+    gridbar(P.cnt, 0);
+
+    const float* Ab  = P.A + (size_t)b * 65536;
+    float* Hb  = P.H + (size_t)b * 32768;
+    float* H2b = P.H2 + (size_t)b * 32768;
+
+    stage_gcn1(S, Ab, Hb, P.rw0, P.rr0, P.rb0, H2b, c0, t, q, u);
+    gridbar(P.cnt, 1);
+    stage_gcn2(S, Ab, H2b, P.ng, P.nbta, P.law0, P.lab0, P.lbw0, P.lbb0, Hb, c0, t, q, u);
+    gridbar(P.cnt, 2);
+    stage_gcn1(S, Ab, Hb, P.rw1, P.rr1, P.rb1, H2b, c0, t, q, u);
+    gridbar(P.cnt, 3);
+    stage_gcn2(S, Ab, H2b, P.ng, P.nbta, P.law1, P.lab1, P.lbw1, P.lbb1, Hb, c0, t, q, u);
+    gridbar(P.cnt, 4);
+
     {
-        float bb = b2[t];
+        const int qd = t & 63, ud = t >> 6;
+        float* Wt   = S;
+        float* hraw = S + 8192;
+        float* ph2  = S + 9216;
+        float* part = S + 11264;
+        float* hmv  = S + 15360;
+        #pragma unroll
+        for (int rnd = 0; rnd < 4; ++rnd) {
+            int idx = rnd * 256 + t;
+            gld16(P.pw1 + idx * 4, &Wt[idx * 4]);
+        }
+        gld16(P.H + (size_t)r0 * 128 + t * 4, &hraw[t * 4]);
+        if (t < 8) hmv[t] = P.hm[r0 + t];
+        __syncthreads();
+        float acc[32];
+        #pragma unroll
+        for (int i = 0; i < 32; ++i) acc[i] = 0.f;
+        #pragma unroll 1
+        for (int kt = 0; kt < 8; ++kt) {
+            const int buf = kt & 1;
+            if (kt < 7) {
+                #pragma unroll
+                for (int rnd = 0; rnd < 4; ++rnd) {
+                    int idx = rnd * 256 + t;
+                    gld16(P.pw1 + (kt + 1) * 4096 + idx * 4,
+                          &Wt[(buf ^ 1) * 4096 + idx * 4]);
+                }
+            }
+            const float* wt = &Wt[buf * 4096];
+            #pragma unroll
+            for (int kk = 0; kk < 4; ++kk) {
+                int kl = ud * 4 + kk;
+                int k  = kt * 16 + kl;
+                float4 w4 = *(const float4*)&wt[kl * 256 + qd * 4];
+                float wc[4] = {w4.x, w4.y, w4.z, w4.w};
+                float hr[8];
+                #pragma unroll
+                for (int r = 0; r < 8; ++r) hr[r] = hraw[r * 128 + k];
+                #pragma unroll
+                for (int r = 0; r < 8; ++r)
+                    #pragma unroll
+                    for (int c = 0; c < 4; ++c)
+                        acc[r * 4 + c] = fmaf(hr[r], wc[c], acc[r * 4 + c]);
+            }
+            __syncthreads();
+        }
+        #pragma unroll
+        for (int gg = 0; gg < 2; ++gg) {
+            #pragma unroll
+            for (int rr = 0; rr < 4; ++rr) {
+                int r = gg * 4 + rr;
+                *(float4*)&part[ud * 1024 + rr * 256 + qd * 4] =
+                    make_float4(acc[r*4+0], acc[r*4+1], acc[r*4+2], acc[r*4+3]);
+            }
+            __syncthreads();
+            #pragma unroll
+            for (int e = 0; e < 4; ++e) {
+                int idx = e * 256 + t;
+                int rr = idx >> 8, f = idx & 255;
+                float s = P.pb1[f];
+                #pragma unroll
+                for (int uu = 0; uu < 4; ++uu) s += part[uu * 1024 + rr * 256 + f];
+                ph2[(gg * 4 + rr) * 256 + f] = fmaxf(s, 0.f);
+            }
+            __syncthreads();
+        }
+        #pragma unroll
+        for (int rnd = 0; rnd < 4; ++rnd) {
+            int idx = rnd * 256 + t;
+            gld16(P.pw2 + idx * 4, &Wt[idx * 4]);
+        }
+        __syncthreads();
+        float a2[32];
+        #pragma unroll
+        for (int i = 0; i < 32; ++i) a2[i] = 0.f;
+        #pragma unroll 1
+        for (int kt = 0; kt < 16; ++kt) {
+            const int buf = kt & 1;
+            if (kt < 15) {
+                #pragma unroll
+                for (int rnd = 0; rnd < 4; ++rnd) {
+                    int idx = rnd * 256 + t;
+                    gld16(P.pw2 + (kt + 1) * 4096 + idx * 4,
+                          &Wt[(buf ^ 1) * 4096 + idx * 4]);
+                }
+            }
+            const float* wt = &Wt[buf * 4096];
+            #pragma unroll
+            for (int kk = 0; kk < 4; ++kk) {
+                int kl = ud * 4 + kk;
+                int k  = kt * 16 + kl;
+                float4 w4 = *(const float4*)&wt[kl * 256 + qd * 4];
+                float wc[4] = {w4.x, w4.y, w4.z, w4.w};
+                float pr[8];
+                #pragma unroll
+                for (int r = 0; r < 8; ++r) pr[r] = ph2[r * 256 + k];
+                #pragma unroll
+                for (int r = 0; r < 8; ++r)
+                    #pragma unroll
+                    for (int c = 0; c < 4; ++c)
+                        a2[r * 4 + c] = fmaf(pr[r], wc[c], a2[r * 4 + c]);
+            }
+            __syncthreads();
+        }
         float hp = 0.f, sp = 0.f;
         #pragma unroll
-        for (int r = 0; r < 8; ++r) {
-            float s = bb;
-            #pragma unroll
-            for (int uu = 0; uu < 4; ++uu) s += part[uu * 2048 + r * 256 + t];
-            float p = fmaxf(s, 0.f);
-            sp += p;
-            hp = fmaf(p, hmv[r], hp);
-        }
-        atomicAdd(&hsum[b * 256 + t], hp);
-        atomicAdd(&asum[b * 256 + t], sp - hp);
-    }
-}
-
-__global__ __launch_bounds__(256) void k_rho(const float* __restrict__ hsum,
-        const float* __restrict__ asum,
-        const float* __restrict__ w1, const float* __restrict__ b1,
-        const float* __restrict__ w2, const float* __restrict__ b2,
-        float* __restrict__ out) {
-    const int bIdx = blockIdx.x;
-    const int t = threadIdx.x, q = t & 31, u = t >> 5;
-    __shared__ __align__(16) float pool[10240];
-    __shared__ __align__(16) float sv[512];
-    __shared__ float wsv[2];
-    float* part = pool + 8192;
-    #pragma unroll
-    for (int rnd = 0; rnd < 4; ++rnd) {
-        int idx = rnd * 256 + t;
-        gld16(w1 + idx * 4, &pool[idx * 4]);
-    }
-    sv[t] = hsum[bIdx * 256 + t];
-    sv[256 + t] = asum[bIdx * 256 + t];
-    __syncthreads();
-    float aH[4] = {0.f, 0.f, 0.f, 0.f}, aA[4] = {0.f, 0.f, 0.f, 0.f};
-    #pragma unroll 1
-    for (int kt = 0; kt < 8; ++kt) {
-        const int buf = kt & 1;
-        if (kt < 7) {
-            #pragma unroll
-            for (int rnd = 0; rnd < 4; ++rnd) {
-                int idx = rnd * 256 + t;
-                gld16(w1 + (kt + 1) * 4096 + idx * 4,
-                      &pool[(buf ^ 1) * 4096 + idx * 4]);
-            }
-        }
-        const float* wt = &pool[buf * 4096];
-        #pragma unroll
-        for (int kk = 0; kk < 4; ++kk) {
-            int kl = u * 4 + kk;
-            int k  = kt * 32 + kl;
-            float4 w4 = *(const float4*)&wt[kl * 128 + q * 4];
-            float sh = sv[k], sa = sv[256 + k];
-            aH[0] = fmaf(sh, w4.x, aH[0]); aA[0] = fmaf(sa, w4.x, aA[0]);
-            aH[1] = fmaf(sh, w4.y, aH[1]); aA[1] = fmaf(sa, w4.y, aA[1]);
-            aH[2] = fmaf(sh, w4.z, aH[2]); aA[2] = fmaf(sa, w4.z, aA[2]);
-            aH[3] = fmaf(sh, w4.w, aH[3]); aA[3] = fmaf(sa, w4.w, aA[3]);
-        }
-        __syncthreads();
-    }
-    *(float4*)&part[u * 256 + q * 4]       = make_float4(aH[0], aH[1], aH[2], aH[3]);
-    *(float4*)&part[u * 256 + 128 + q * 4] = make_float4(aA[0], aA[1], aA[2], aA[3]);
-    __syncthreads();
-    if (t < 64) {
-        int vec = t >> 5, fq = t & 31;
-        float4 s = make_float4(0.f, 0.f, 0.f, 0.f);
-        #pragma unroll
-        for (int uu = 0; uu < 8; ++uu) {
-            float4 p = *(const float4*)&part[uu * 256 + vec * 128 + fq * 4];
-            s.x += p.x; s.y += p.y; s.z += p.z; s.w += p.w;
-        }
-        float4 bb = *(const float4*)&b1[fq * 4];
-        float4 w2q = *(const float4*)&w2[fq * 4];
-        float p = fmaxf(s.x + bb.x, 0.f) * w2q.x
-                + fmaxf(s.y + bb.y, 0.f) * w2q.y
-                + fmaxf(s.z + bb.z, 0.f) * w2q.z
-                + fmaxf(s.w + bb.w, 0.f) * w2q.w;
-        #pragma unroll
-        for (int o = 16; o > 0; o >>= 1) p += __shfl_down(p, o, 32);
-        if ((t & 31) == 0) wsv[vec] = p;
-    }
-    __syncthreads();
-    if (t == 0) out[bIdx] = 0.5f + 0.5f * tanhf(wsv[0] - wsv[1]);
+        for (int gg = 0; gg < 2; ++gg) {
+            #pragma unroll
+            for (int rr = 0; rr < 4; ++rr) {
+                int r = gg * 4 + rr;
+                *(float4*)&part[ud * 1024 + rr * 256 + qd * 4] =
+                    make_float4(a2[r*4+0], a2[r*4+1], a2[r*4+2], a2[r*4+3]);
+            }
+            __syncthreads();
+            {
+                float bb = P.pb2[t];
+                #pragma unroll
+                for (int rr = 0; rr < 4; ++rr) {
+                    float s = bb;
+                    #pragma unroll
+                    for (int uu = 0; uu < 4; ++uu) s += part[uu * 1024 + rr * 256 + t];
+                    float p = fmaxf(s, 0.f);
+                    sp += p;
+                    hp = fmaf(p, hmv[gg * 4 + rr], hp);
+                }
+            }
+            __syncthreads();
+        }
+        atomicAdd(&P.hsum[b * 256 + t], hp);
+        atomicAdd(&P.asum[b * 256 + t], sp - hp);
+    }
+    gridbar(P.cnt, 5);
+
+    if (blk < NB) {
+        float* Wt   = S;
+        float* sv   = S + 8192;
+        float* part = S + 8704;
+        float* wsv  = S + 10752;
+        #pragma unroll
+        for (int rnd = 0; rnd < 4; ++rnd) {
+            int idx = rnd * 256 + t;
+            gld16(P.qw1 + idx * 4, &Wt[idx * 4]);
+        }
+        sv[t]       = P.hsum[blk * 256 + t];
+        sv[256 + t] = P.asum[blk * 256 + t];
+        __syncthreads();
+        float aH[4] = {0.f, 0.f, 0.f, 0.f}, aA[4] = {0.f, 0.f, 0.f, 0.f};
+        #pragma unroll 1
+        for (int kt = 0; kt < 8; ++kt) {
+            const int buf = kt & 1;
+            if (kt < 7) {
+                #pragma unroll
+                for (int rnd = 0; rnd < 4; ++rnd) {
+                    int idx = rnd * 256 + t;
+                    gld16(P.qw1 + (kt + 1) * 4096 + idx * 4,
+                          &Wt[(buf ^ 1) * 4096 + idx * 4]);
+                }
+            }
+            const float* wt = &Wt[buf * 4096];
+            #pragma unroll
+            for (int kk = 0; kk < 4; ++kk) {
+                int kl = u * 4 + kk;
+                int k  = kt * 32 + kl;
+                float4 w4 = *(const float4*)&wt[kl * 128 + q * 4];
+                float sh = sv[k], sa = sv[256 + k];
+                aH[0] = fmaf(sh, w4.x, aH[0]); aA[0] = fmaf(sa, w4.x, aA[0]);
+                aH[1] = fmaf(sh, w4.y, aH[1]); aA[1] = fmaf(sa, w4.y, aA[1]);
+                aH[2] = fmaf(sh, w4.z, aH[2]); aA[2] = fmaf(sa, w4.z, aA[2]);
+                aH[3] = fmaf(sh, w4.w, aH[3]); aA[3] = fmaf(sa, w4.w, aA[3]);
+            }
+            __syncthreads();
+        }
+        *(float4*)&part[u * 256 + q * 4]       = make_float4(aH[0], aH[1], aH[2], aH[3]);
+        *(float4*)&part[u * 256 + 128 + q * 4] = make_float4(aA[0], aA[1], aA[2], aA[3]);
+        __syncthreads();
+        if (t < 64) {
+            int vec = t >> 5, fq = t & 31;
+            float4 s = make_float4(0.f, 0.f, 0.f, 0.f);
+            #pragma unroll
+            for (int uu = 0; uu < 8; ++uu) {
+                float4 p = *(const float4*)&part[uu * 256 + vec * 128 + fq * 4];
+                s.x += p.x; s.y += p.y; s.z += p.z; s.w += p.w;
+            }
+            float4 bb  = *(const float4*)&P.qb1[fq * 4];
+            float4 w2q = *(const float4*)&P.qw2[fq * 4];
+            float p = fmaxf(s.x + bb.x, 0.f) * w2q.x
+                    + fmaxf(s.y + bb.y, 0.f) * w2q.y
+                    + fmaxf(s.z + bb.z, 0.f) * w2q.z
+                    + fmaxf(s.w + bb.w, 0.f) * w2q.w;
+            #pragma unroll
+            for (int o = 16; o > 0; o >>= 1) p += __shfl_down(p, o, 32);
+            if ((t & 31) == 0) wsv[vec] = p;
+        }
+        __syncthreads();
+        if (t == 0)
+            P.outp[blk] = 0.5f + 0.5f * tanhf(wsv[0] - wsv[1]);
+    }
 }
 
 extern "C" void kernel_launch(void* const* d_in, const int* in_sizes, int n_in,
                               void* d_out, int out_size, void* d_ws, size_t ws_size,
                               hipStream_t stream) {
-    const float* A         = (const float*)d_in[0];
-    const float* X         = (const float*)d_in[1];
-    const float* home_mask = (const float*)d_in[2];
-    const float* emb1_w    = (const float*)d_in[3];
-    const float* emb1_b    = (const float*)d_in[4];
-    const float* emb2_w    = (const float*)d_in[5];
-    const float* emb2_b    = (const float*)d_in[6];
-    const float* rgcn_w[2]    = { (const float*)d_in[7],  (const float*)d_in[14] };
-    const float* rgcn_root[2] = { (const float*)d_in[8],  (const float*)d_in[15] };
-    const float* rgcn_bias[2] = { (const float*)d_in[9],  (const float*)d_in[16] };
-    const float* lina_w[2]    = { (const float*)d_in[10], (const float*)d_in[17] };
-    const float* lina_b[2]    = { (const float*)d_in[11], (const float*)d_in[18] };
-    const float* linb_w[2]    = { (const float*)d_in[12], (const float*)d_in[19] };
-    const float* linb_b[2]    = { (const float*)d_in[13], (const float*)d_in[20] };
-    const float* norm_g  = (const float*)d_in[21];
-    const float* norm_b  = (const float*)d_in[22];
-    const float* phi_w1  = (const float*)d_in[23];
-    const float* phi_b1  = (const float*)d_in[24];
-    const float* phi_w2  = (const float*)d_in[25];
-    const float* phi_b2  = (const float*)d_in[26];
-    const float* rho_w1  = (const float*)d_in[27];
-    const float* rho_b1  = (const float*)d_in[28];
-    const float* rho_w2  = (const float*)d_in[29];
-    const float* rho_b2  = (const float*)d_in[30];
-    float* out = (float*)d_out;
-
-    float* ws   = (float*)d_ws;
-    float* H    = ws;
-    float* H2   = ws + 262144;
-    float* hsum = ws + 524288;
-    float* asum = ws + 526336;
-
-    k_embed<<<512, 256, 0, stream>>>(X, emb1_w, emb1_b, emb2_w, emb2_b, H, hsum);
-
-    for (int it = 0; it < 2; ++it) {
-        k_gcn1<<<512, 256, 0, stream>>>(A, H, rgcn_w[it], rgcn_root[it],
-                                        rgcn_bias[it], H2);
-        k_gcn2<<<512, 256, 0, stream>>>(A, H2, norm_g, norm_b,
-                                        lina_w[it], lina_b[it],
-                                        linb_w[it], linb_b[it], H);
-    }
-
-    k_deepset<<<256, 256, 0, stream>>>(H, home_mask, phi_w1, phi_b1,
-                                       phi_w2, phi_b2, hsum, asum);
-    k_rho<<<NB, 256, 0, stream>>>(hsum, asum, rho_w1, rho_b1, rho_w2, rho_b2, out);
+    float* ws = (float*)d_ws;
+    Params P;
+    P.A    = (const float*)d_in[0];
+    P.X    = (const float*)d_in[1];
+    P.hm   = (const float*)d_in[2];
+    P.e1w  = (const float*)d_in[3];
+    P.e1b  = (const float*)d_in[4];
+    P.e2w  = (const float*)d_in[5];
+    P.e2b  = (const float*)d_in[6];
+    P.rw0  = (const float*)d_in[7];
+    P.rr0  = (const float*)d_in[8];
+    P.rb0  = (const float*)d_in[9];
+    P.law0 = (const float*)d_in[10];
+    P.lab0 = (const float*)d_in[11];
+    P.lbw0 = (const float*)d_in[12];
+    P.lbb0 = (const float*)d_in[13];
+    P.rw1  = (const float*)d_in[14];
+    P.rr1  = (const float*)d_in[15];
+    P.rb1  = (const float*)d_in[16];
+    P.law1 = (const float*)d_in[17];
+    P.lab1 = (const float*)d_in[18];
+    P.lbw1 = (const float*)d_in[19];
+    P.lbb1 = (const float*)d_in[20];
+    P.ng   = (const float*)d_in[21];
+    P.nbta = (const float*)d_in[22];
+    P.pw1  = (const float*)d_in[23];
+    P.pb1  = (const float*)d_in[24];
+    P.pw2  = (const float*)d_in[25];
+    P.pb2  = (const float*)d_in[26];
+    P.qw1  = (const float*)d_in[27];
+    P.qb1  = (const float*)d_in[28];
+    P.qw2  = (const float*)d_in[29];
+    P.qb2  = (const float*)d_in[30];
+    P.H    = ws;
+    P.H2   = ws + 262144;
+    P.hsum = ws + 524288;
+    P.asum = ws + 526336;
+    P.cnt  = (int*)(ws + 528384);
+    P.outp = (float*)d_out;
+
+    k_init<<<17, 256, 0, stream>>>(P.hsum, P.cnt);
+    k_mega<<<GRID, 256, 0, stream>>>(P);
 }
```
